# Kernel optimization log

Measured on AMD Instinct MI355X. Metric: run time of the kernel, lower is better.

Reference implementation:

```python
import jax, jax.numpy as jnp
import numpy as np
from jax import lax
from jax.scipy.linalg import cho_solve, solve_triangular

T_LEN, D, K = 8192, 32, 16
LOG2PI = float(np.log(2.0 * np.pi))


def setup_inputs():
    ks = jax.random.split(jax.random.key(0), 14)
    R = 0.1 * jax.random.normal(ks[0], (T_LEN, D, D))
    recog_J = jnp.einsum('tij,tkj->tik', R, R) + 0.5 * jnp.eye(D)  # SPD recognition precisions
    recog_h = 0.1 * jax.random.normal(ks[1], (T_LEN, D, 1))
    loc = 0.1 * jax.random.normal(ks[2], (D, 1))
    Tau_p = jnp.eye(D) + 0.05 * jax.random.normal(ks[3], (D, D))
    Lambda_p = jnp.eye(D) + 0.05 * jax.random.normal(ks[4], (D, D))
    X = 0.9 * jnp.eye(D, D + 1) + 0.05 * jax.random.normal(ks[5], (D, D + 1))
    init_lps = jax.nn.log_softmax(jax.random.normal(ks[6], (K,)))[:, None]
    trans_lps = jax.nn.log_softmax(jax.random.normal(ks[7], (K, K)), axis=1)
    Rp = 0.1 * jax.random.normal(ks[8], (K, D, D))
    prior_lam = jnp.einsum('kij,klj->kil', Rp, Rp) + jnp.eye(D)
    prior_X = 0.9 * jnp.eye(D, D + 1) + 0.05 * jax.random.normal(ks[9], (K, D, D + 1))
    Rt = 0.1 * jax.random.normal(ks[10], (D, D))
    prior_tau = Rt @ Rt.T + jnp.eye(D)
    prior_mu = 0.1 * jax.random.normal(ks[11], (D, 1))
    init_lps_prior = jax.nn.log_softmax(jax.random.normal(ks[12], (K,)))[:, None]
    trans_lps_prior = jax.nn.log_softmax(jax.random.normal(ks[13], (K, K)), axis=1)
    return dict(recog_J=recog_J, recog_h=recog_h, loc=loc, Tau_p=Tau_p, Lambda_p=Lambda_p, X=X,
                init_lps=init_lps, trans_lps=trans_lps, prior_lam=prior_lam, prior_X=prior_X,
                prior_tau=prior_tau, prior_mu=prior_mu, init_lps_prior=init_lps_prior,
                trans_lps_prior=trans_lps_prior, seed=42)


def _slds(recog_J, recog_h, loc, Tau_p, Lambda_p, X, init_lps, trans_lps,
          prior_lam, prior_X, prior_tau, prior_mu, init_lps_prior, trans_lps_prior, seed):
    Dd = loc.shape[0]
    Kk = init_lps.shape[0]
    Tt = recog_J.shape[0]
    Nn = Tt - 1
    eye = jnp.eye(Dd, dtype=recog_J.dtype)
    jitter = 1e-6 * eye

    # expected_params: inference LDS natural params
    tau = Tau_p @ Tau_p.T + 1e-8 * eye
    tau_mu = tau @ loc
    lam = Lambda_p @ Lambda_p.T + 1e-8 * eye
    A = X[:, :Dd]
    b = X[:, Dd:]
    ATlam = A.T @ lam
    ATlamA = ATlam @ A
    lamA = lam @ A
    lamb = lam @ b
    ATlamb = A.T @ lamb
    bTlamb = (b.T @ lamb)[0, 0]
    logdet_lam = jnp.linalg.slogdet(lam)[1]

    # ---- HMM forward-backward over z_{1:N} (emissions are zeros, kept general) ----
    emit = jnp.zeros((Nn, Kk), dtype=recog_J.dtype)

    def fstep(a, e):
        a2 = jax.nn.logsumexp(a[:, None] + trans_lps, axis=0) + e
        return a2, a2
    a0 = init_lps[:, 0] + emit[0]
    _, alphas_rest = lax.scan(fstep, a0, emit[1:])
    alphas = jnp.concatenate([a0[None], alphas_rest], 0)  # (N,K)
    hmm_logZ = jax.nn.logsumexp(alphas[-1])

    def bstep(beta_next, e_next):
        beta = jax.nn.logsumexp(trans_lps + (e_next + beta_next)[None, :], axis=1)
        return beta, beta
    _, betas_head = lax.scan(bstep, jnp.zeros(Kk, dtype=recog_J.dtype), emit[1:], reverse=True)
    betas = jnp.concatenate([betas_head, jnp.zeros((1, Kk), dtype=recog_J.dtype)], 0)
    cat_es = jnp.exp(alphas + betas - hmm_logZ)  # (N,K) marginals q(z_t)
    pair = jnp.exp(alphas[:-1, :, None] + trans_lps[None] + (emit[1:] + betas[1:])[:, None, :] - hmm_logZ)
    EZZNT = jnp.sum(pair, 0)  # (K,K) expected transition counts

    hmm_kl = (jnp.sum(cat_es[0] * (init_lps[:, 0] - init_lps_prior[:, 0]))
              + jnp.sum(EZZNT * (trans_lps - trans_lps_prior))
              + jnp.sum(cat_es * emit) - hmm_logZ)

    # ---- LDS information-form Kalman filter (computes logZ of q) ----
    J0 = tau + recog_J[0]
    h0 = tau_mu + recog_h[0]
    logc0 = -0.5 * (loc.T @ tau_mu)[0, 0] + 0.5 * jnp.linalg.slogdet(tau)[1] - 0.5 * Dd * LOG2PI

    def filt(carry, xs):
        J, h, lc = carry
        Jr, hr = xs
        M = J + ATlamA + jitter
        C = jnp.linalg.cholesky(M)
        u = h - ATlamb
        Minv_u = cho_solve((C, True), u)
        logdetM = 2.0 * jnp.sum(jnp.log(jnp.diagonal(C)))
        Jn = lam + Jr - lamA @ cho_solve((C, True), ATlam)
        hn = lamb + hr + lamA @ Minv_u
        lc = lc - 0.5 * bTlamb + 0.5 * logdet_lam + 0.5 * (u.T @ Minv_u)[0, 0] - 0.5 * logdetM
        return (Jn, hn, lc), (Jn, hn)

    (Jlast, hlast, logc), (Jf_rest, hf_rest) = lax.scan(filt, (J0, h0, logc0), (recog_J[1:], recog_h[1:]))
    Jf = jnp.concatenate([J0[None], Jf_rest], 0)  # (T,D,D) filtered precisions
    hf = jnp.concatenate([h0[None], hf_rest], 0)  # (T,D,1)
    Cl = jnp.linalg.cholesky(Jlast + jitter)
    mlast = cho_solve((Cl, True), hlast)
    logZq = logc + 0.5 * (hlast.T @ mlast)[0, 0] + 0.5 * Dd * LOG2PI - jnp.sum(jnp.log(jnp.diagonal(Cl)))

    # ---- RTS smoother -> gaussian expected stats ----
    CovT = cho_solve((Cl, True), eye)

    def smooth(carry, xs):
        m_n, Cov_n = carry
        Jt, ht = xs
        P = Jt + ATlamA + jitter
        C = jnp.linalg.cholesky(P)
        G = cho_solve((C, True), ATlam)
        g = cho_solve((C, True), ht - ATlamb)
        m = G @ m_n + g
        Pinv = cho_solve((C, True), eye)
        Cov = Pinv + G @ Cov_n @ G.T
        cross = G @ (Cov_n + m_n @ m_n.T) + g @ m_n.T  # E[x_t x_{t+1}^T]
        return (m, Cov), (m, Cov, cross)

    _, (m_head, Cov_head, cross) = lax.scan(smooth, (mlast, CovT), (Jf[:-1], hf[:-1]), reverse=True)
    Ex = jnp.concatenate([m_head, mlast[None]], 0)  # (T,D,1)
    Cov = jnp.concatenate([Cov_head, CovT[None]], 0)
    ExxT = Cov + jnp.einsum('tiz,tjz->tij', Ex, Ex)  # (T,D,D)
    Cross = jnp.swapaxes(cross, 1, 2)  # E[x_{t+1} x_t^T], (N,D,D)
    Ex2 = Ex[..., 0]

    # ---- E_q[log p_inf(x)] ----
    init_term = (-0.5 * jnp.einsum('ij,ij->', tau, ExxT[0]) + jnp.dot(Ex2[0], tau_mu[:, 0])
                 - 0.5 * (loc.T @ tau_mu)[0, 0] + 0.5 * jnp.linalg.slogdet(tau)[1] - 0.5 * Dd * LOG2PI)
    trans_term = (-0.5 * jnp.einsum('ij,nij->', lam, ExxT[1:])
                  + jnp.einsum('ij,nij->', lamA, Cross)
                  - 0.5 * jnp.einsum('ij,nij->', ATlamA, ExxT[:-1])
                  + jnp.einsum('i,ni->', lamb[:, 0], Ex2[1:])
                  - jnp.einsum('i,ni->', ATlamb[:, 0], Ex2[:-1])
                  + Nn * (-0.5 * bTlamb + 0.5 * logdet_lam - 0.5 * Dd * LOG2PI))
    E_log_p_inf = init_term + trans_term

    # ---- hmm_to_lds_mf: mixture (mean-field) prior expected log-density ----
    Ak = prior_X[:, :, :Dd]
    bk = prior_X[:, :, Dd:]
    lamAk = jnp.einsum('kij,kjl->kil', prior_lam, Ak)
    ATlamAk = jnp.einsum('kji,kjl->kil', Ak, lamAk)
    lambk = jnp.einsum('kij,kjz->kiz', prior_lam, bk)
    ATlambk = jnp.einsum('kji,kjz->kiz', Ak, lambk)
    bTlambk = jnp.einsum('kjz,kjz->k', bk, lambk)
    logdetk = jnp.linalg.slogdet(prior_lam)[1]
    w = cat_es  # (N,K)
    mix_trans = (-0.5 * jnp.einsum('nk,kij,nij->', w, prior_lam, ExxT[1:])
                 + jnp.einsum('nk,kij,nij->', w, lamAk, Cross)
                 - 0.5 * jnp.einsum('nk,kij,nij->', w, ATlamAk, ExxT[:-1])
                 + jnp.einsum('nk,ki,ni->', w, lambk[:, :, 0], Ex2[1:])
                 - jnp.einsum('nk,ki,ni->', w, ATlambk[:, :, 0], Ex2[:-1])
                 + jnp.einsum('nk,k->', w, -0.5 * bTlambk + 0.5 * logdetk)
                 - 0.5 * Nn * Dd * LOG2PI)
    tpm = prior_tau @ prior_mu
    mix_init = (-0.5 * jnp.einsum('ij,ij->', prior_tau, ExxT[0]) + jnp.dot(Ex2[0], tpm[:, 0])
                - 0.5 * (prior_mu.T @ tpm)[0, 0] + 0.5 * jnp.linalg.slogdet(prior_tau)[1] - 0.5 * Dd * LOG2PI)
    E_log_p_mix = mix_init + mix_trans

    recog_term = (-0.5 * jnp.einsum('tij,tij->', recog_J, ExxT)
                  + jnp.einsum('tiz,tiz->', recog_h, Ex))
    lds_kl = E_log_p_inf + recog_term - logZq - E_log_p_mix

    # ---- joint backward sampling of x_{1:T} ~ q ----
    eps = jax.random.normal(jax.random.fold_in(jax.random.key(seed), 1), (Tt, Dd, 1), dtype=recog_J.dtype)
    xT = mlast + solve_triangular(Cl.T, eps[-1], lower=False)

    def samp(x_next, xs):
        Jt, ht, e = xs
        P = Jt + ATlamA + jitter
        C = jnp.linalg.cholesky(P)
        mean = cho_solve((C, True), ht - ATlamb + ATlam @ x_next)
        x = mean + solve_triangular(C.T, e, lower=False)
        return x, x

    _, xs_head = lax.scan(samp, xT, (Jf[:-1], hf[:-1], eps[:-1]), reverse=True)
    z = jnp.concatenate([xs_head, xT[None]], 0)[..., 0]  # (T,D)

    return z, Ex, ExxT, Cross, cat_es, lds_kl + hmm_kl


def reference(recog_J, recog_h, loc, Tau_p, Lambda_p, X, init_lps, trans_lps,
              prior_lam, prior_X, prior_tau, prior_mu, init_lps_prior, trans_lps_prior, seed):
    return _slds(recog_J, recog_h, loc, Tau_p, Lambda_p, X, init_lps, trans_lps,
                 prior_lam, prior_X, prior_tau, prior_mu, init_lps_prior, trans_lps_prior, seed)
```

## Files before the change

### kernel.cpp

```cpp
#include <hip/hip_runtime.h>
#include <math.h>
#include <stdint.h>

#define Dd 32
#define TT 8192
#define NN 8191
#define KK 16
#define LOG2PI_ 1.8378770664093453

#define WSD_LOGC0  0
#define WSD_LOGZQ  1
#define WSD_MIXC   3
#define WSD_LDLAM  4
#define WSD_BTLAMB 5
#define WSD_PR     8
#define WSD_PT     1032
#define WSD_PM     2056
#define F_TAU      0
#define F_TAUMU    1024
#define F_LAM      1056
#define F_A        2080
#define F_B        3104
#define F_ATLAM    3136
#define F_ATLAMA   4160
#define F_LAMA     5184
#define F_LAMB     6208
#define F_ATLAMB   6240
#define F_SC       6272
#define F_LAMAK    6304
#define F_ATLAMAK  22688
#define F_LAMBK    39072
#define F_ATLAMBK  39584
#define F_BTLAMBK  40096
#define F_LOGDETK  40112
#define F_TPM      40128
#define F_J0       40160
#define F_H0       41184
#define F_MLAST    41216
#define F_COVT     41248
#define F_XT       42272
#define F_TPOW     42304
#define F_ALPHA    45632
#define F_BETA     176704
#define F_EZ       307776
#define F_SCAN     340544

#define SSTR   2148
#define POFF   0
#define QOFF   528
#define ROFF   1056
#define PPOFF  2080
#define QQOFF  2112
#define GAMOFF 2144
#define FLGOFF 2146
#define BG     0
#define BCZ    1024
#define BCM    1056
#define BP     1088

#define O_Z     ((size_t)0)
#define O_EX    ((size_t)262144)
#define O_EXXT  ((size_t)524288)
#define O_CROSS ((size_t)8912896)
#define O_CAT   ((size_t)17300480)
#define O_KL    ((size_t)17431536)

__device__ __forceinline__ uint32_t rotl32(uint32_t v, int d){ return (v<<d)|(v>>(32-d)); }
__device__ __forceinline__ void threefry2x32(uint32_t k0, uint32_t k1, uint32_t x0, uint32_t x1,
                                             uint32_t& o0, uint32_t& o1){
  uint32_t ks2 = k0 ^ k1 ^ 0x1BD11BDAu;
  x0 += k0; x1 += k1;
  x0+=x1; x1=rotl32(x1,13); x1^=x0;  x0+=x1; x1=rotl32(x1,15); x1^=x0;
  x0+=x1; x1=rotl32(x1,26); x1^=x0;  x0+=x1; x1=rotl32(x1, 6); x1^=x0;
  x0+=k1; x1+=ks2+1u;
  x0+=x1; x1=rotl32(x1,17); x1^=x0;  x0+=x1; x1=rotl32(x1,29); x1^=x0;
  x0+=x1; x1=rotl32(x1,16); x1^=x0;  x0+=x1; x1=rotl32(x1,24); x1^=x0;
  x0+=ks2; x1+=k0+2u;
  x0+=x1; x1=rotl32(x1,13); x1^=x0;  x0+=x1; x1=rotl32(x1,15); x1^=x0;
  x0+=x1; x1=rotl32(x1,26); x1^=x0;  x0+=x1; x1=rotl32(x1, 6); x1^=x0;
  x0+=k0; x1+=k1+3u;
  x0+=x1; x1=rotl32(x1,17); x1^=x0;  x0+=x1; x1=rotl32(x1,29); x1^=x0;
  x0+=x1; x1=rotl32(x1,16); x1^=x0;  x0+=x1; x1=rotl32(x1,24); x1^=x0;
  x0+=k1; x1+=ks2+4u;
  x0+=x1; x1=rotl32(x1,13); x1^=x0;  x0+=x1; x1=rotl32(x1,15); x1^=x0;
  x0+=x1; x1=rotl32(x1,26); x1^=x0;  x0+=x1; x1=rotl32(x1, 6); x1^=x0;
  x0+=ks2; x1+=k0+5u;
  o0=x0; o1=x1;
}
__device__ __forceinline__ float tf_normal(uint32_t bits){
  float fl = __uint_as_float((bits>>9) | 0x3F800000u) - 1.0f;
  const float lo = -0.99999994f;
  float u = fmaxf(lo, fl*2.0f + lo);
  float w = -log1pf(-u*u);
  float p;
  if (w < 5.0f){
    w -= 2.5f;
    p = 2.81022636e-08f;
    p = fmaf(p,w,3.43273939e-07f); p = fmaf(p,w,-3.5233877e-06f);
    p = fmaf(p,w,-4.39150654e-06f); p = fmaf(p,w,0.00021858087f);
    p = fmaf(p,w,-0.00125372503f); p = fmaf(p,w,-0.00417768164f);
    p = fmaf(p,w,0.246640727f); p = fmaf(p,w,1.50140941f);
  } else {
    w = sqrtf(w) - 3.0f;
    p = -0.000200214257f;
    p = fmaf(p,w,0.000100950558f); p = fmaf(p,w,0.00134934322f);
    p = fmaf(p,w,-0.00367342844f); p = fmaf(p,w,0.00573950773f);
    p = fmaf(p,w,-0.0076224613f); p = fmaf(p,w,0.00943887047f);
    p = fmaf(p,w,1.00167406f); p = fmaf(p,w,2.83297682f);
  }
  return 1.4142135381698608f * (p*u);
}

__device__ __forceinline__ void tri_rc(int i, int& r, int& c){
  int rr = (int)((sqrtf(8.f*(float)i+1.f)-1.f)*0.5f);
  while((rr+1)*(rr+2)/2 <= i) ++rr;
  while(rr*(rr+1)/2 > i) --rr;
  r = rr; c = i - rr*(rr+1)/2;
}

__device__ __forceinline__ float dot36(const float* A, int r, const float* B, int c){
  const float4* a4 = (const float4*)(A + r*36);
  const float4* b4 = (const float4*)(B + c*36);
  float sx=0.f, sy=0.f, sz=0.f, sw=0.f;
  #pragma unroll
  for(int m=0;m<8;++m){
    float4 a=a4[m], b=b4[m];
    sx=fmaf(a.x,b.x,sx); sy=fmaf(a.y,b.y,sy);
    sz=fmaf(a.z,b.z,sz); sw=fmaf(a.w,b.w,sw);
  }
  return (sx+sy)+(sz+sw);
}
__device__ __forceinline__ void t36_rows(float* dst, const float* src, int tid){
  int r=tid>>3, c0=(tid&7)<<2;
  *(float4*)(dst + r*36 + c0) = *(const float4*)(src + r*32 + c0);
}
__device__ __forceinline__ void t36_tr(float* dst, const float* src, int tid){
  int m=tid>>3, j0=(tid&7)<<2;
  float4 v = *(const float4*)(src + m*32 + j0);
  dst[(j0+0)*36+m]=v.x; dst[(j0+1)*36+m]=v.y;
  dst[(j0+2)*36+m]=v.z; dst[(j0+3)*36+m]=v.w;
}
__device__ __forceinline__ void t36_tr36(float* dst, const float* src, int tid){
  int m=tid>>3, j0=(tid&7)<<2;
  float4 v = *(const float4*)(src + m*36 + j0);
  dst[(j0+0)*36+m]=v.x; dst[(j0+1)*36+m]=v.y;
  dst[(j0+2)*36+m]=v.z; dst[(j0+3)*36+m]=v.w;
}
__device__ __forceinline__ void t36_sym(float* dst, const float* packed, int tid){
  for(int q=tid;q<528;q+=256){
    int r,c; tri_rc(q,r,c);
    float v=packed[q];
    dst[r*36+c]=v; dst[c*36+r]=v;
  }
}

__device__ double chol_linv36(float* W, float* Li, float* rdg, int tid){
  int r = tid>>3, c0 = (tid&7)<<2;
  {
    float4 z = make_float4(0.f,0.f,0.f,0.f);
    if(r>=c0 && r<c0+4) ((float*)&z)[r-c0]=1.f;
    *(float4*)(Li + r*36 + c0) = z;
  }
  double slog=0.0;
  for(int j=0;j<33;++j){
    if(j<32){
      float dd = W[j*36+j];
      float rd = 1.0f/sqrtf(dd);
      float invd = rd*rd;
      if(tid==0){ rdg[j]=rd; slog += (double)(0.5f*__logf(dd)); }
      if(r>j && c0+3>=j){
        float t0 = W[j*36+r]*invd;
        float4 wj  = *(const float4*)(W+j*36+c0);
        float4 cur = *(float4*)(W+r*36+c0);
        float rdl = rd;
        int c;
        c=c0;   cur.x = (c>j)? fmaf(-t0, wj.x, cur.x) : ((c==j)? cur.x*rdl : cur.x);
        c=c0+1; cur.y = (c>j)? fmaf(-t0, wj.y, cur.y) : ((c==j)? cur.y*rdl : cur.y);
        c=c0+2; cur.z = (c>j)? fmaf(-t0, wj.z, cur.z) : ((c==j)? cur.z*rdl : cur.z);
        c=c0+3; cur.w = (c>j)? fmaf(-t0, wj.w, cur.w) : ((c==j)? cur.w*rdl : cur.w);
        *(float4*)(W+r*36+c0) = cur;
      }
    }
    if(j>0){
      int ii=j-1;
      if(r>ii && c0<=ii){
        float wri = W[r*36+ii]*rdg[ii];
        float4 lrow = *(const float4*)(Li+ii*36+c0);
        float4 cur  = *(float4*)(Li+r*36+c0);
        if(c0+0<=ii) cur.x = fmaf(-wri, lrow.x, cur.x);
        if(c0+1<=ii) cur.y = fmaf(-wri, lrow.y, cur.y);
        if(c0+2<=ii) cur.z = fmaf(-wri, lrow.z, cur.z);
        if(c0+3<=ii) cur.w = fmaf(-wri, lrow.w, cur.w);
        *(float4*)(Li+r*36+c0) = cur;
      }
    }
    __syncthreads();
  }
  {
    float rr = rdg[r];
    float4 cur = *(float4*)(Li+r*36+c0);
    cur.x*=rr; cur.y*=rr; cur.z*=rr; cur.w*=rr;
    *(float4*)(Li+r*36+c0) = cur;
  }
  __syncthreads();
  return slog;
}

__device__ __forceinline__ double blk_red(double v, double* sd, int tid){
  sd[tid]=v; __syncthreads();
  for(int s=128;s>0;s>>=1){ if(tid<s) sd[tid]+=sd[tid+s]; __syncthreads(); }
  double r=sd[0]; __syncthreads(); return r;
}
__device__ double blk_logdet(float* Ms, int tid){
  double sl = 0.0;
  for (int j=0;j<Dd;++j){
    float dd = Ms[j*33+j];
    sl += log((double)dd);
    float invd = 1.0f/dd;
    #pragma unroll
    for(int p=0;p<4;p++){
      int cell = tid + (p<<8); int r=cell>>5, c=cell&31;
      if(r>j && c>j && c<=r) Ms[r*33+c] -= Ms[r*33+j]*(Ms[c*33+j]*invd);
    }
    __syncthreads();
  }
  return sl;
}

__device__ void gen_leaf(float* S, int s, const float* rJ, const float* rh,
                         const float* wsf, const double* wsd, int tid){
  if(s==0){
    #pragma unroll 3
    for(int q=tid;q<528;q+=256){
      int r,c; tri_rc(q,r,c);
      S[POFF+q]=0.f;
      S[QOFF+q]=wsf[F_J0 + r*32+c];
    }
    #pragma unroll 4
    for(int q=tid;q<1024;q+=256) S[ROFF+q]=0.f;
    if(tid<32){ S[PPOFF+tid]=0.f; S[QQOFF+tid]=wsf[F_H0+tid]; }
    if(tid==0){ *(double*)(S+GAMOFF)=wsd[WSD_LOGC0]; S[FLGOFF]=1.f; }
  } else {
    #pragma unroll 3
    for(int q=tid;q<528;q+=256){
      int r,c; tri_rc(q,r,c);
      S[POFF+q] = wsf[F_ATLAMA + r*32+c] + ((r==c)?1e-6f:0.f);
      S[QOFF+q] = wsf[F_LAM + r*32+c] + rJ[(size_t)s*1024 + r*32+c];
    }
    #pragma unroll 4
    for(int q=tid;q<1024;q+=256) S[ROFF+q] = -wsf[F_ATLAM+q];
    if(tid<32){
      S[PPOFF+tid] = -wsf[F_ATLAMB+tid];
      S[QQOFF+tid] = wsf[F_LAMB+tid] + rh[(size_t)s*32+tid];
    }
    if(tid==0){
      *(double*)(S+GAMOFF) = -0.5*wsd[WSD_BTLAMB] + 0.5*wsd[WSD_LDLAM];
      S[FLGOFF]=1.f;
    }
  }
}

__global__ __launch_bounds__(256) void k_setup(const float* rJ, const float* rh, const float* loc,
    const float* Tp, const float* Lp, const float* X, const float* plam, const float* pX,
    const float* ptau, const float* pmu, float* wsf, double* wsd){
  __shared__ float s1[1056], s2[1056], s3[1056];
  __shared__ float sv[32], sv2[32];
  int tid=threadIdx.x; int b=blockIdx.x;
  if(b==0){
    for(int p=0;p<4;p++){int cell=tid+(p<<8);int r=cell>>5,c=cell&31; s1[r*33+c]=Tp[cell];}
    if(tid<32) sv[tid]=loc[tid];
    __syncthreads();
    for(int p=0;p<4;p++){int cell=tid+(p<<8);int r=cell>>5,c=cell&31;
      float a=0.f;
      #pragma unroll
      for(int m=0;m<Dd;++m) a=fmaf(s1[r*33+m], s1[c*33+m], a);
      if(r==c) a+=1e-8f;
      s2[r*33+c]=a; wsf[F_TAU+cell]=a; wsf[F_J0+cell]=a+rJ[cell];
    }
    __syncthreads();
    if(tid<32){ float tm=0.f;
      #pragma unroll
      for(int m=0;m<Dd;++m) tm=fmaf(s2[tid*33+m], sv[m], tm);
      sv2[tid]=tm; wsf[F_TAUMU+tid]=tm; wsf[F_H0+tid]=tm+rh[tid];
    }
    __syncthreads();
    double ldt = blk_logdet(s2, tid);
    if(tid==0){ double dd=0; for(int m=0;m<Dd;++m) dd += (double)sv[m]*(double)sv2[m];
      wsd[WSD_LOGC0] = -0.5*dd + 0.5*ldt - 0.5*Dd*LOG2PI_; }
  } else if(b==1){
    for(int p=0;p<4;p++){int cell=tid+(p<<8);int r=cell>>5,c=cell&31; s1[r*33+c]=Lp[cell];}
    __syncthreads();
    for(int p=0;p<4;p++){int cell=tid+(p<<8);int r=cell>>5,c=cell&31;
      float a=0.f;
      #pragma unroll
      for(int m=0;m<Dd;++m) a=fmaf(s1[r*33+m], s1[c*33+m], a);
      if(r==c) a+=1e-8f;
      s2[r*33+c]=a; wsf[F_LAM+cell]=a;
    }
    __syncthreads();
    for(int p=0;p<4;p++){int cell=tid+(p<<8);int r=cell>>5,c=cell&31;
      float a=X[r*33+c]; s3[r*33+c]=a; wsf[F_A+cell]=a; }
    if(tid<32){ sv[tid]=X[tid*33+32]; wsf[F_B+tid]=sv[tid]; }
    __syncthreads();
    for(int p=0;p<4;p++){int cell=tid+(p<<8);int r=cell>>5,c=cell&31;
      float a=0.f,b2=0.f;
      #pragma unroll
      for(int m=0;m<Dd;++m){ a=fmaf(s2[r*33+m], s3[m*33+c], a); b2=fmaf(s3[m*33+r], s2[m*33+c], b2); }
      s1[r*33+c]=a; wsf[F_LAMA+cell]=a; wsf[F_ATLAM+cell]=b2;
    }
    if(tid<32){ float lb=0.f;
      #pragma unroll
      for(int m=0;m<Dd;++m) lb=fmaf(s2[tid*33+m], sv[m], lb);
      sv2[tid]=lb; wsf[F_LAMB+tid]=lb;
    }
    __syncthreads();
    for(int p=0;p<4;p++){int cell=tid+(p<<8);int r=cell>>5,c=cell&31;
      float a=0.f;
      #pragma unroll
      for(int m=0;m<Dd;++m) a=fmaf(s3[m*33+r], s1[m*33+c], a);
      wsf[F_ATLAMA+cell]=a;
    }
    if(tid<32){ float ab=0.f;
      #pragma unroll
      for(int m=0;m<Dd;++m) ab=fmaf(s3[m*33+tid], sv2[m], ab);
      wsf[F_ATLAMB+tid]=ab;
    }
    if(tid==0){ double bb=0; for(int m=0;m<Dd;++m) bb += (double)sv[m]*(double)sv2[m];
      wsd[WSD_BTLAMB]=bb; }
    __syncthreads();
    double ldl = blk_logdet(s2, tid);
    if(tid==0) wsd[WSD_LDLAM]=ldl;
  } else if(b==2){
    for(int p=0;p<4;p++){int cell=tid+(p<<8);int r=cell>>5,c=cell&31; s1[r*33+c]=ptau[cell];}
    if(tid<32) sv[tid]=pmu[tid];
    __syncthreads();
    if(tid<32){ float tm=0.f;
      #pragma unroll
      for(int m=0;m<Dd;++m) tm=fmaf(s1[tid*33+m], sv[m], tm);
      sv2[tid]=tm; wsf[F_TPM+tid]=tm;
    }
    __syncthreads();
    double ldp = blk_logdet(s1, tid);
    if(tid==0){ double dd=0; for(int m=0;m<Dd;++m) dd += (double)sv[m]*(double)sv2[m];
      wsd[WSD_MIXC] = -0.5*dd + 0.5*ldp - 0.5*Dd*LOG2PI_; }
  } else {
    int k2 = b-3;
    for(int p=0;p<4;p++){int cell=tid+(p<<8);int r=cell>>5,c=cell&31;
      s2[r*33+c]=plam[k2*1024+cell]; s3[r*33+c]=pX[k2*1056 + r*33 + c];}
    if(tid<32) sv[tid]=pX[k2*1056 + tid*33 + 32];
    __syncthreads();
    for(int p=0;p<4;p++){int cell=tid+(p<<8);int r=cell>>5,c=cell&31;
      float a=0.f;
      #pragma unroll
      for(int m=0;m<Dd;++m) a=fmaf(s2[r*33+m], s3[m*33+c], a);
      s1[r*33+c]=a; wsf[F_LAMAK + (size_t)k2*1024 + cell]=a;
    }
    if(tid<32){ float lb=0.f;
      #pragma unroll
      for(int m=0;m<Dd;++m) lb=fmaf(s2[tid*33+m], sv[m], lb);
      sv2[tid]=lb; wsf[F_LAMBK + k2*32 + tid]=lb;
    }
    __syncthreads();
    for(int p=0;p<4;p++){int cell=tid+(p<<8);int r=cell>>5,c=cell&31;
      float a=0.f;
      #pragma unroll
      for(int m=0;m<Dd;++m) a=fmaf(s3[m*33+r], s1[m*33+c], a);
      wsf[F_ATLAMAK + (size_t)k2*1024 + cell]=a;
    }
    if(tid<32){ float ab=0.f;
      #pragma unroll
      for(int m=0;m<Dd;++m) ab=fmaf(s3[m*33+tid], sv2[m], ab);
      wsf[F_ATLAMBK + k2*32 + tid]=ab;
    }
    if(tid==0){ float bb=0.f; for(int m=0;m<Dd;++m) bb=fmaf(sv[m],sv2[m],bb);
      wsf[F_BTLAMBK + k2]=bb; }
    __syncthreads();
    double dk = blk_logdet(s2, tid);
    if(tid==0) wsf[F_LOGDETK + k2]=(float)dk;
  }
}

__global__ __launch_bounds__(256) void k_eps(const int* seedp, float* outz){
  uint32_t seed = (uint32_t)seedp[0];
  uint32_t K0,K1;
  threefry2x32(0u, seed, 0u, 1u, K0, K1);
  uint32_t i = blockIdx.x*256u + threadIdx.x;
  uint32_t o0,o1;
  threefry2x32(K0, K1, 0u, i, o0, o1);
  outz[i] = tf_normal(o0 ^ o1);
}

__global__ __launch_bounds__(256) void k_hmmpow(const float* tl, float* wsf){
  __shared__ float A0[256], A1[256];
  int tid=threadIdx.x;
  A0[tid]=tl[tid];
  wsf[F_TPOW+tid]=A0[tid];
  __syncthreads();
  float* cur=A0; float* nxt=A1;
  for(int k=1;k<13;++k){
    int i=tid>>4, j=tid&15;
    float mx=-3.0e38f;
    #pragma unroll
    for(int m=0;m<16;++m) mx=fmaxf(mx, cur[i*16+m]+cur[m*16+j]);
    float s=0.f;
    #pragma unroll
    for(int m=0;m<16;++m) s+=__expf(cur[i*16+m]+cur[m*16+j]-mx);
    float v=mx+__logf(s);
    nxt[tid]=v; wsf[F_TPOW+k*256+tid]=v;
    __syncthreads();
    float* t2=cur; cur=nxt; nxt=t2;
  }
}

__global__ __launch_bounds__(256) void k_hmmab(const float* il, float* wsf){
  __shared__ float S[3328];
  int tid=threadIdx.x;
  for(int p=0;p<13;++p) S[p*256+tid]=wsf[F_TPOW+p*256+tid];
  __syncthreads();
  int n = blockIdx.x*256 + tid;
  if(n>NN-1) return;
  float v[16], w[16];
  #pragma unroll
  for(int j=0;j<16;++j) v[j]=il[j];
  for(int k=0;k<13;++k){
    if((n>>k)&1){
      #pragma unroll
      for(int j=0;j<16;++j){
        float mx=-3.0e38f;
        #pragma unroll
        for(int i2=0;i2<16;++i2) mx=fmaxf(mx, v[i2]+S[k*256+i2*16+j]);
        float s=0.f;
        #pragma unroll
        for(int i2=0;i2<16;++i2) s+=__expf(v[i2]+S[k*256+i2*16+j]-mx);
        w[j]=mx+__logf(s);
      }
      #pragma unroll
      for(int j=0;j<16;++j) v[j]=w[j];
    }
  }
  #pragma unroll
  for(int j=0;j<16;++j) wsf[F_ALPHA+(size_t)n*16+j]=v[j];
  if(n==NN-1){
    float mx=-3.0e38f;
    #pragma unroll
    for(int j=0;j<16;++j) mx=fmaxf(mx,v[j]);
    float s=0.f;
    #pragma unroll
    for(int j=0;j<16;++j) s+=__expf(v[j]-mx);
    wsf[F_SC+0]=mx+__logf(s);
  }
  int m = NN-1-n;
  float b[16];
  #pragma unroll
  for(int i2=0;i2<16;++i2) b[i2]=0.f;
  for(int k=0;k<13;++k){
    if((m>>k)&1){
      #pragma unroll
      for(int i2=0;i2<16;++i2){
        float mx=-3.0e38f;
        #pragma unroll
        for(int j=0;j<16;++j) mx=fmaxf(mx, S[k*256+i2*16+j]+b[j]);
        float s=0.f;
        #pragma unroll
        for(int j=0;j<16;++j) s+=__expf(S[k*256+i2*16+j]+b[j]-mx);
        w[i2]=mx+__logf(s);
      }
      #pragma unroll
      for(int i2=0;i2<16;++i2) b[i2]=w[i2];
    }
  }
  #pragma unroll
  for(int i2=0;i2<16;++i2) wsf[F_BETA+(size_t)n*16+i2]=b[i2];
}

__global__ __launch_bounds__(256) void k_cat(const float* tl, float* wsf, float* out){
  __shared__ float Ts[256]; __shared__ float al[1024]; __shared__ float be[1040];
  int tid=threadIdx.x;
  Ts[tid]=tl[tid];
  float logZ = wsf[F_SC+0];
  int n0=blockIdx.x*64;
  for(int q=tid;q<1024;q+=256){ int n=n0+(q>>4); al[q] = (n<NN)? wsf[F_ALPHA+(size_t)n*16+(q&15)] : 0.f; }
  for(int q=tid;q<1040;q+=256){ int n=n0+(q>>4); be[q] = (n<NN)? wsf[F_BETA +(size_t)n*16+(q&15)] : 0.f; }
  __syncthreads();
  for(int q=tid;q<1024;q+=256){ int n=n0+(q>>4);
    if(n<NN) out[O_CAT+(size_t)n*16+(q&15)] = __expf(al[q]+be[q]-logZ); }
  int i=tid>>4, j=tid&15;
  float acc=0.f;
  #pragma unroll 4
  for(int nn=0;nn<64;++nn){
    int n=n0+nn;
    if(n<NN-1) acc += __expf(al[nn*16+i]+Ts[i*16+j]+be[(nn+1)*16+j]-logZ);
  }
  wsf[F_EZ + blockIdx.x*256 + tid]=acc;
}

__global__ __launch_bounds__(256,4) void k_cf(const float* rJ, const float* rh,
    float* wsf, double* wsd, float* out, int d, int mode){
  __shared__ __align__(16) float SA[2148], SB[2148];
  __shared__ __align__(16) float W[1152], Li[1152], BA[1152], BB[1152];
  __shared__ float rdg[32], Ls[32];
  int tid = threadIdx.x;
  int i = blockIdx.x;
  int iA = (i<<(d+1)) + (1<<d) - 1;
  int iB = iA + (1<<d);
  float* base = wsf + F_SCAN;
  float* pa = base + (size_t)iA*SSTR;
  float* pb = base + (size_t)iB*SSTR;
  if(d==0){
    gen_leaf(SA, iA, rJ, rh, wsf, wsd, tid);
    if(mode==0) gen_leaf(SB, iB, rJ, rh, wsf, wsd, tid);
    else { 
      #pragma unroll 3
      for(int q=tid;q<537;q+=256) ((float4*)SB)[q]=((const float4*)pb)[q];
    }
  } else {
    #pragma unroll 3
    for(int q=tid;q<537;q+=256){ ((float4*)SA)[q]=((const float4*)pa)[q]; ((float4*)SB)[q]=((const float4*)pb)[q]; }
  }
  __syncthreads();
  int fa=(SA[FLGOFF]!=0.f), fb=(SB[FLGOFF]!=0.f);
  if(mode==1){
    float* st = out + O_EXXT;
    #pragma unroll 3
    for(int q=tid;q<537;q+=256){ ((float4*)st)[q]=((float4*)SB)[q]; ((float4*)pb)[q]=((float4*)SA)[q]; }
    if(tid==0) pa[FLGOFF]=0.f;
    return;
  }
  if(mode==2){
    #pragma unroll 3
    for(int q=tid;q<537;q+=256) ((float4*)pa)[q]=((float4*)SB)[q];
  }
  float* X = (mode==2)? SB : SA;  int fx=(mode==2)?fb:fa;
  float* Y = (mode==2)? SA : SB;  int fy=(mode==2)?fa:fb;
  if(!fx && !fy){ if(tid==0) pb[FLGOFF]=0.f; return; }
  if(!fx){ 
    #pragma unroll 3
    for(int q=tid;q<537;q+=256) ((float4*)pb)[q]=((float4*)Y)[q]; return; }
  if(!fy){ 
    #pragma unroll 3
    for(int q=tid;q<537;q+=256) ((float4*)pb)[q]=((float4*)X)[q]; return; }
  #pragma unroll 3
  for(int q=tid;q<528;q+=256){
    int r,c; tri_rc(q,r,c);
    float w = X[QOFF+q] + Y[POFF+q];
    W[r*36+c]=w; W[c*36+r]=w;
  }
  t36_rows(BA, X+ROFF, tid);
  t36_tr  (BB, Y+ROFF, tid);
  __syncthreads();
  double slog = chol_linv36(W, Li, rdg, tid);
  if(tid<32){
    float acc=0.f;
    for(int m=0;m<=tid;++m) acc = fmaf(Li[tid*36+m], X[QQOFF+m]+Y[PPOFF+m], acc);
    Ls[tid]=acc;
  }
  #pragma unroll 4
  for(int q=tid;q<1024;q+=256){
    int i2=q>>5, j=q&31;
    W[j*36+i2] = dot36(Li, i2, BA, j);
  }
  __syncthreads();
  #pragma unroll 4
  for(int q=tid;q<1024;q+=256){
    int i2=q>>5, j=q&31;
    BA[j*36+i2] = dot36(Li, i2, BB, j);
  }
  __syncthreads();
  #pragma unroll 3
  for(int q=tid;q<528;q+=256){
    int r,c; tri_rc(q,r,c);
    pb[POFF+q] = X[POFF+q] - dot36(W, r, W, c);
    pb[QOFF+q] = Y[QOFF+q] - dot36(BA, r, BA, c);
  }
  #pragma unroll 4
  for(int q=tid;q<1024;q+=256){
    int r=q>>5, c=q&31;
    pb[ROFF+q] = -dot36(W, r, BA, c);
  }
  if(tid<32){
    float ap=0.f,aq=0.f;
    #pragma unroll
    for(int m=0;m<32;++m){ ap=fmaf(W[tid*36+m],Ls[m],ap); aq=fmaf(BA[tid*36+m],Ls[m],aq); }
    pb[PPOFF+tid] = X[PPOFF+tid] - ap;
    pb[QQOFF+tid] = Y[QQOFF+tid] - aq;
  }
  if(tid==0){
    double g = *(double*)(X+GAMOFF) + *(double*)(Y+GAMOFF);
    double dot=0.0;
    for(int m=0;m<32;++m) dot += (double)Ls[m]*(double)Ls[m];
    *(double*)(pb+GAMOFF) = g + 0.5*dot - slog;
    pb[FLGOFF]=1.f;
  }
}

__global__ __launch_bounds__(256,6) void k_point(float* wsf, double* wsd, float* out){
  __shared__ __align__(16) float SE[2148];
  __shared__ __align__(16) float W[1152], Li[1152], AUX[1152];
  __shared__ float rdg[32], uv[32], Lu[32], ev[32], gv[32], yv[32];
  int tid=threadIdx.x; int b=blockIdx.x;
  float* base = wsf + F_SCAN;
  float* outz = out + O_Z;
  if(b>0){
    int t = b-1;
    float* pe = base + (size_t)b*SSTR;
    #pragma unroll 3
    for(int q=tid;q<537;q+=256) ((float4*)SE)[q]=((const float4*)pe)[q];
    if(tid<32) ev[tid]=outz[(size_t)t*32+tid];
    t36_rows(AUX, wsf+F_LAMA, tid);
    __syncthreads();
    #pragma unroll 3
    for(int q=tid;q<528;q+=256){
      int r,c; tri_rc(q,r,c);
      float w = SE[QOFF+q] + wsf[F_ATLAMA + r*32+c] + ((r==c)?1e-6f:0.f);
      W[r*36+c]=w; W[c*36+r]=w;
    }
    if(tid<32) uv[tid]=SE[QQOFF+tid]-wsf[F_ATLAMB+tid];
    __syncthreads();
    chol_linv36(W, Li, rdg, tid);
    if(tid<32){
      float acc=0.f;
      for(int m=0;m<=tid;++m) acc=fmaf(Li[tid*36+m],uv[m],acc);
      Lu[tid]=acc;
    }
    #pragma unroll 4
    for(int q=tid;q<1024;q+=256){
      int i2=q>>5, j=q&31;
      W[j*36+i2] = dot36(Li, i2, AUX, j);
    }
    __syncthreads();
    t36_tr36(AUX, Li, tid);
    if(tid<32){
      float ag=0.f, ay=0.f;
      for(int m2=tid;m2<32;++m2){ float lv=Li[m2*36+tid]; ag=fmaf(lv,Lu[m2],ag); ay=fmaf(lv,ev[m2],ay); }
      gv[tid]=ag; yv[tid]=ay;
    }
    __syncthreads();
    #pragma unroll 4
    for(int q=tid;q<1024;q+=256){
      int r=q>>5,c=q&31;
      pe[BG+q] = dot36(AUX, r, W, c);
    }
    float* outc = out + O_CROSS + (size_t)t*1024;
    #pragma unroll 3
    for(int q=tid;q<528;q+=256){
      int r,c; tri_rc(q,r,c);
      float a = dot36(AUX, r, AUX, c);
      pe[BP+q]=a; outc[q]=a;
    }
    if(tid<32){
      pe[BCM+tid]=gv[tid]; pe[BCZ+tid]=gv[tid]+yv[tid]; outc[528+tid]=gv[tid];
    }
    if(tid==0) pe[FLGOFF]=1.f;
  } else {
    const float* st = out + O_EXXT;
    #pragma unroll 3
    for(int q=tid;q<537;q+=256) ((float4*)SE)[q]=((const float4*)st)[q];
    if(tid<32) ev[tid]=outz[(size_t)NN*32+tid];
    __syncthreads();
    for(int q=tid;q<528;q+=256){
      int r,c; tri_rc(q,r,c);
      float w = SE[QOFF+q] + ((r==c)?1e-6f:0.f);
      W[r*36+c]=w; W[c*36+r]=w;
    }
    if(tid<32) uv[tid]=SE[QQOFF+tid];
    __syncthreads();
    double slog2 = chol_linv36(W, Li, rdg, tid);
    if(tid<32){
      float acc=0.f;
      for(int m=0;m<=tid;++m) acc=fmaf(Li[tid*36+m],uv[m],acc);
      Lu[tid]=acc;
    }
    t36_tr36(AUX, Li, tid);
    __syncthreads();
    if(tid<32){
      float am=0.f, ay=0.f;
      for(int m2=tid;m2<32;++m2){ float lv=Li[m2*36+tid]; am=fmaf(lv,Lu[m2],am); ay=fmaf(lv,ev[m2],ay); }
      gv[tid]=am; yv[tid]=ay;
      wsf[F_MLAST+tid]=am; out[O_EX+(size_t)NN*32+tid]=am;
      float xt=am+ay;
      wsf[F_XT+tid]=xt; out[O_Z+(size_t)NN*32+tid]=xt;
    }
    __syncthreads();
    for(int q=tid;q<1024;q+=256){
      int r=q>>5,c=q&31;
      float a = dot36(AUX, r, AUX, c);
      wsf[F_COVT+q]=a;
      out[O_EXXT+(size_t)NN*1024+q]=a+gv[r]*gv[c];
    }
    if(tid==0){
      double gam=*(const double*)(SE+GAMOFF);
      double hm=0.0;
      for(int m=0;m<32;++m) hm += (double)uv[m]*(double)gv[m];
      wsd[WSD_LOGZQ] = gam + 0.5*hm + 0.5*Dd*LOG2PI_ - slog2;
    }
  }
}

__device__ __forceinline__ int amap(int j){ return (j<NN)? (NN-j) : 0; }

__global__ __launch_bounds__(256,4) void k_ca(float* wsf, int d, int mode){
  __shared__ __align__(16) float SA[2148], SB[2148];
  __shared__ __align__(16) float GY36[1152], GB[1152], PX36[1152];
  int tid = threadIdx.x;
  int i = blockIdx.x;
  int iA = (i<<(d+1)) + (1<<d) - 1;
  int iB = iA + (1<<d);
  float* base = wsf + F_SCAN;
  float* pa = base + (size_t)amap(iA)*SSTR;
  float* pb = base + (size_t)amap(iB)*SSTR;
  #pragma unroll 3
  for(int q=tid;q<537;q+=256){ ((float4*)SA)[q]=((const float4*)pa)[q]; ((float4*)SB)[q]=((const float4*)pb)[q]; }
  __syncthreads();
  int fa=(SA[FLGOFF]!=0.f), fb=(SB[FLGOFF]!=0.f);
  if(mode==1){
    #pragma unroll 3
    for(int q=tid;q<537;q+=256) ((float4*)pb)[q]=((float4*)SA)[q];
    if(tid==0) pa[FLGOFF]=0.f;
    return;
  }
  if(mode==2){
    #pragma unroll 3
    for(int q=tid;q<537;q+=256) ((float4*)pa)[q]=((float4*)SB)[q];
  }
  float* X = (mode==2)? SB : SA;  int fx=(mode==2)?fb:fa;
  float* Y = (mode==2)? SA : SB;  int fy=(mode==2)?fa:fb;
  if(!fx && !fy){ if(tid==0) pb[FLGOFF]=0.f; return; }
  if(!fx){ 
    #pragma unroll 3
    for(int q=tid;q<537;q+=256) ((float4*)pb)[q]=((float4*)Y)[q]; return; }
  if(!fy){ 
    #pragma unroll 3
    for(int q=tid;q<537;q+=256) ((float4*)pb)[q]=((float4*)X)[q]; return; }
  t36_rows(GY36, Y+BG, tid);
  t36_tr  (GB,   X+BG, tid);
  t36_sym (PX36, X+BP, tid);
  __syncthreads();
  #pragma unroll 4
  for(int q=tid;q<1024;q+=256){
    int r=q>>5,c=q&31;
    pb[BG+q] = dot36(GY36, r, GB, c);
  }
  __syncthreads();
  #pragma unroll 4
  for(int q=tid;q<1024;q+=256){
    int r=q>>5,c=q&31;
    GB[r*36+c] = dot36(GY36, r, PX36, c);
  }
  __syncthreads();
  #pragma unroll 3
  for(int q=tid;q<528;q+=256){
    int r,c; tri_rc(q,r,c);
    pb[BP+q] = dot36(GB, r, GY36, c) + Y[BP+q];
  }
  if(tid<32){
    float az=0.f,am=0.f;
    #pragma unroll
    for(int m=0;m<32;++m){ float g=GY36[tid*36+m]; az=fmaf(g,X[BCZ+m],az); am=fmaf(g,X[BCM+m],am); }
    pb[BCZ+tid]=az+Y[BCZ+tid];
    pb[BCM+tid]=am+Y[BCM+tid];
  }
  if(tid==0) pb[FLGOFF]=1.f;
}

__global__ __launch_bounds__(256,6) void k_smz(float* wsf, float* out){
  __shared__ __align__(16) float G36[1152], CV36[1152], Tm36[1152];
  __shared__ float mlv[32], xtv[32], mv[32], zv[32];
  int tid=threadIdx.x;
  int t = blockIdx.x;
  const float* pe = wsf + F_SCAN + (size_t)t*SSTR;
  t36_rows(G36,  pe+BG,       tid);
  t36_rows(CV36, wsf+F_COVT,  tid);
  if(tid<32){ mlv[tid]=wsf[F_MLAST+tid]; xtv[tid]=wsf[F_XT+tid]; }
  __syncthreads();
  if(tid<32){
    float am=0.f, az=0.f;
    #pragma unroll
    for(int m=0;m<32;++m){
      float g=G36[tid*36+m];
      am=fmaf(g, mlv[m], am);
      az=fmaf(g, xtv[m], az);
    }
    mv[tid]=am+pe[BCM+tid];
    zv[tid]=az+pe[BCZ+tid];
    out[O_EX+(size_t)t*32+tid]=mv[tid];
    out[O_Z +(size_t)t*32+tid]=zv[tid];
  }
  #pragma unroll 4
  for(int q=tid;q<1024;q+=256){
    int r=q>>5,c=q&31;
    Tm36[r*36+c] = dot36(G36, r, CV36, c);
  }
  __syncthreads();
  #pragma unroll 3
  for(int q=tid;q<528;q+=256){
    int r,c; tri_rc(q,r,c);
    float cov = dot36(Tm36, r, G36, c) + pe[BP+q];
    float e = cov + mv[r]*mv[c];
    out[O_EXXT+(size_t)t*1024 + r*32+c]=e;
    if(r!=c) out[O_EXXT+(size_t)t*1024 + c*32+r]=e;
  }
}

__global__ __launch_bounds__(256,6) void k_cross(float* wsf, float* out){
  __shared__ __align__(16) float PV36[1152], LA36[1152], E136[1152], GF36[1152];
  __shared__ float gv[32], m1[32];
  int tid=threadIdx.x;
  int t = blockIdx.x;
  float* outc = out + O_CROSS + (size_t)t*1024;
  t36_sym (PV36, outc, tid);
  t36_rows(LA36, wsf+F_LAMA, tid);
  t36_rows(E136, out+O_EXXT+(size_t)(t+1)*1024, tid);
  if(tid<32){ gv[tid]=outc[528+tid]; m1[tid]=out[O_EX+(size_t)(t+1)*32+tid]; }
  __syncthreads();
  #pragma unroll 4
  for(int q=tid;q<1024;q+=256){
    int r=q>>5,c=q&31;
    GF36[r*36+c] = dot36(PV36, r, LA36, c);
  }
  __syncthreads();
  #pragma unroll 4
  for(int q=tid;q<1024;q+=256){
    int i2=q>>5, j=q&31;
    float acc = dot36(GF36, j, E136, i2);
    outc[q] = acc + gv[j]*m1[i2];
  }
}

__global__ __launch_bounds__(256) void k_terms(const float* rJ, const float* rh,
    const float* plam, float* wsf, double* wsd, float* out){
  __shared__ float slam[1056], slamA[1056], sata[1056];
  __shared__ float slamb[32], satlb[32], cst[16], sw[16];
  __shared__ double sd[256];
  int tid=threadIdx.x; int i8=tid>>3, c4=(tid&7)*4;
  for(int p=0;p<4;p++){int cell=tid+(p<<8);int r=cell>>5,c=cell&31;
    slam[r*33+c]=wsf[F_LAM+cell]; slamA[r*33+c]=wsf[F_LAMA+cell]; sata[r*33+c]=wsf[F_ATLAMA+cell];}
  if(tid<32){slamb[tid]=wsf[F_LAMB+tid]; satlb[tid]=wsf[F_ATLAMB+tid];}
  if(tid<16) cst[tid] = -0.5f*wsf[F_BTLAMBK+tid] + 0.5f*wsf[F_LOGDETK+tid];
  __syncthreads();
  double dr=0.0, dt=0.0, dm=0.0;
  int t0=blockIdx.x*8;
  for(int tt=0;tt<8;++tt){
    int t=t0+tt;
    if(t<NN){ if(tid<16) sw[tid]=out[O_CAT+(size_t)t*16+tid]; }
    __syncthreads();
    size_t cb=(size_t)t*1024+((size_t)i8<<5)+c4;
    float4 exT=*(const float4*)(out+O_EXXT+cb);
    float4 rj =*(const float4*)(rJ+cb);
    dr += -0.5*(double)(rj.x*exT.x+rj.y*exT.y+rj.z*exT.z+rj.w*exT.w);
    if(tid<32) dr += (double)(rh[(size_t)t*32+tid]*out[O_EX+(size_t)t*32+tid]);
    if(t>=1){
      dt += -0.5*(double)(slam[i8*33+c4]*exT.x + slam[i8*33+c4+1]*exT.y
                        + slam[i8*33+c4+2]*exT.z + slam[i8*33+c4+3]*exT.w);
      if(tid<32) dt += (double)(slamb[tid]*out[O_EX+(size_t)t*32+tid]);
    }
    if(t<NN){
      float4 crT =*(const float4*)(out+O_CROSS+cb);
      float4 exT1=*(const float4*)(out+O_EXXT+cb+1024);
      dt += (double)(slamA[i8*33+c4]*crT.x + slamA[i8*33+c4+1]*crT.y
                   + slamA[i8*33+c4+2]*crT.z + slamA[i8*33+c4+3]*crT.w)
          -0.5*(double)(sata[i8*33+c4]*exT.x + sata[i8*33+c4+1]*exT.y
                      + sata[i8*33+c4+2]*exT.z + sata[i8*33+c4+3]*exT.w);
      if(tid<32) dt -= (double)(satlb[tid]*out[O_EX+(size_t)t*32+tid]);
      const float* pe1=(const float*)&exT1; const float* pcr=(const float*)&crT; const float* pe0=(const float*)&exT;
      #pragma unroll
      for(int q=0;q<4;q++){
        int cc=(i8<<5)+c4+q;
        float wl=0.f, wa=0.f, wt2=0.f;
        #pragma unroll
        for(int k2=0;k2<KK;k2++){ float wv=sw[k2];
          wl =fmaf(wv, plam[(size_t)k2*1024+cc], wl);
          wa =fmaf(wv, wsf[F_LAMAK+(size_t)k2*1024+cc], wa);
          wt2=fmaf(wv, wsf[F_ATLAMAK+(size_t)k2*1024+cc], wt2);}
        dm += (double)(-0.5f*wl*pe1[q] + wa*pcr[q] - 0.5f*wt2*pe0[q]);
      }
      if(tid<32){
        float wlb=0.f, wtb=0.f;
        #pragma unroll
        for(int k2=0;k2<KK;k2++){ wlb=fmaf(sw[k2], wsf[F_LAMBK+k2*32+tid], wlb);
                                  wtb=fmaf(sw[k2], wsf[F_ATLAMBK+k2*32+tid], wtb);}
        dm += (double)(wlb*out[O_EX+(size_t)(t+1)*32+tid] - wtb*out[O_EX+(size_t)t*32+tid]);
      }
      if(tid<16) dm += (double)(sw[tid]*cst[tid]);
    }
    __syncthreads();
  }
  double r1=blk_red(dr,sd,tid);
  double r2=blk_red(dt,sd,tid);
  double r3=blk_red(dm,sd,tid);
  if(tid==0){ wsd[WSD_PR+blockIdx.x]=r1; wsd[WSD_PT+blockIdx.x]=r2; wsd[WSD_PM+blockIdx.x]=r3; }
}

__global__ __launch_bounds__(256) void k_final(const float* il, const float* tl,
    const float* ilp, const float* tlp, const float* ptau, float* wsf, double* wsd, float* out){
  __shared__ double sd[256];
  int tid=threadIdx.x;
  double ez=0.0;
  for(int b=0;b<128;++b) ez += (double)wsf[F_EZ + b*256 + tid];
  double v = ez * (double)(tl[tid]-tlp[tid]);
  if(tid<16) v += (double)out[O_CAT+tid] * (double)(il[tid]-ilp[tid]);
  double hmmkl = blk_red(v, sd, tid) - (double)wsf[F_SC+0];
  double a=0,b2=0,c=0;
  for(int q=0;q<4;q++){int b3=tid+q*256; a+=wsd[WSD_PR+b3]; b2+=wsd[WSD_PT+b3]; c+=wsd[WSD_PM+b3];}
  double recog=blk_red(a,sd,tid), trns=blk_red(b2,sd,tid), mixt=blk_red(c,sd,tid);
  double ia=0, ib=0, va=0, vb=0;
  for(int p=0;p<4;p++){int cell=tid+(p<<8);
    float e0=out[O_EXXT+cell];
    ia += (double)(wsf[F_TAU+cell]*e0);
    ib += (double)(ptau[cell]*e0);
  }
  if(tid<32){ float ex0=out[O_EX+tid];
    va=(double)(ex0*wsf[F_TAUMU+tid]); vb=(double)(ex0*wsf[F_TPM+tid]); }
  double s_ia=blk_red(ia,sd,tid), s_ib=blk_red(ib,sd,tid);
  double s_va=blk_red(va,sd,tid), s_vb=blk_red(vb,sd,tid);
  if(tid==0){
    double init_term = -0.5*s_ia + s_va + wsd[WSD_LOGC0];
    double mix_init  = -0.5*s_ib + s_vb + wsd[WSD_MIXC];
    double trans_term = trns + (double)NN*(-0.5*wsd[WSD_BTLAMB] + 0.5*wsd[WSD_LDLAM] - 0.5*Dd*LOG2PI_);
    double mix_trans  = mixt - 0.5*(double)NN*(double)Dd*LOG2PI_;
    double lds_kl = (init_term+trans_term) + recog - wsd[WSD_LOGZQ] - (mix_init+mix_trans);
    out[O_KL] = (float)(lds_kl + hmmkl);
  }
}

extern "C" void kernel_launch(void* const* d_in, const int* in_sizes, int n_in,
                              void* d_out, int out_size, void* d_ws, size_t ws_size,
                              hipStream_t stream){
  const float* rJ  =(const float*)d_in[0];
  const float* rh  =(const float*)d_in[1];
  const float* loc =(const float*)d_in[2];
  const float* Tp  =(const float*)d_in[3];
  const float* Lp  =(const float*)d_in[4];
  const float* X   =(const float*)d_in[5];
  const float* il  =(const float*)d_in[6];
  const float* tl  =(const float*)d_in[7];
  const float* plam=(const float*)d_in[8];
  const float* pX  =(const float*)d_in[9];
  const float* ptau=(const float*)d_in[10];
  const float* pmu =(const float*)d_in[11];
  const float* ilp =(const float*)d_in[12];
  const float* tlp =(const float*)d_in[13];
  const int*   seed=(const int*)d_in[14];
  float* out=(float*)d_out;
  double* wsd=(double*)d_ws;
  float* wsf=(float*)((char*)d_ws + 32768);

  k_setup<<<19,256,0,stream>>>(rJ,rh,loc,Tp,Lp,X,plam,pX,ptau,pmu,wsf,wsd);
  k_eps<<<1024,256,0,stream>>>(seed, out + O_Z);
  k_hmmpow<<<1,256,0,stream>>>(tl, wsf);
  k_hmmab<<<32,256,0,stream>>>(il, wsf);
  k_cat<<<128,256,0,stream>>>(tl, wsf, out);
  for(int d=0; d<13; ++d) k_cf<<<(8192>>(d+1)),256,0,stream>>>(rJ, rh, wsf, wsd, out, d, 0);
  k_cf<<<1,256,0,stream>>>(rJ, rh, wsf, wsd, out, 12, 1);
  for(int d=11; d>=0; --d) k_cf<<<(8192>>(d+1)),256,0,stream>>>(rJ, rh, wsf, wsd, out, d, 2);
  k_point<<<8192,256,0,stream>>>(wsf, wsd, out);
  for(int d=0; d<13; ++d) k_ca<<<(8192>>(d+1)),256,0,stream>>>(wsf, d, 0);
  k_ca<<<1,256,0,stream>>>(wsf, 12, 1);
  for(int d=11; d>=0; --d) k_ca<<<(8192>>(d+1)),256,0,stream>>>(wsf, d, 2);
  k_smz<<<NN,256,0,stream>>>(wsf, out);
  k_cross<<<NN,256,0,stream>>>(wsf, out);
  k_terms<<<1024,256,0,stream>>>(rJ, rh, plam, wsf, wsd, out);
  k_final<<<1,256,0,stream>>>(il, tl, ilp, tlp, ptau, wsf, wsd, out);
}
```

Before: 2.077 ms.

## Replace tree scans with chunked three-level blocked scans for filter and smoother

Replaces the up-sweep/down-sweep tree parallel scans (about 25 launches each) for the forward filter and the backward smoother with a blocked scan. Each block first sequentially combines a chunk of 8 elements, then two reduction levels and a single-block exclusive scan of 16 hyper-aggregates run, and finally the prefixes propagate back down. The point-wise k_point and k_smz kernels are fused into the propagation kernels, and scratch prefixes are staged in the O_CROSS output region. This cuts launch count and global traffic but serialises more work per block, with fewer blocks at the middle levels.

```diff
diff --git a/kernel.cpp b/kernel.cpp
--- a/kernel.cpp
+++ b/kernel.cpp
@@ -65,6 +65,10 @@
 #define O_CAT   ((size_t)17300480)
 #define O_KL    ((size_t)17431536)
 
+#define SAGG0  0
+#define SSUP0  1024
+#define SHYP0  1152
+
 __device__ __forceinline__ uint32_t rotl32(uint32_t v, int d){ return (v<<d)|(v>>(32-d)); }
 __device__ __forceinline__ void threefry2x32(uint32_t k0, uint32_t k1, uint32_t x0, uint32_t x1,
                                              uint32_t& o0, uint32_t& o1){
@@ -154,6 +158,29 @@
   }
 }
 
+__device__ __forceinline__ void ld_slot(float* dst, const float* src, int tid){
+  #pragma unroll 3
+  for(int q=tid;q<537;q+=256) ((float4*)dst)[q] = ((const float4*)src)[q];
+}
+__device__ __forceinline__ void st_slot(float* dst, const float* src, int tid){
+  #pragma unroll 3
+  for(int q=tid;q<537;q+=256) ((float4*)dst)[q] = ((const float4*)src)[q];
+}
+__device__ __forceinline__ void st_pref(float* cb, int p, const float* C, int tid){
+  #pragma unroll 3
+  for(int q=tid;q<537;q+=256){
+    int w=q/116, o=(q-116*w)<<2;
+    *(float4*)(cb + (((size_t)(5*p+w))<<10) + 560 + o) = ((const float4*)C)[q];
+  }
+}
+__device__ __forceinline__ void ld_pref(float* C, const float* cb, int p, int tid){
+  #pragma unroll 3
+  for(int q=tid;q<537;q+=256){
+    int w=q/116, o=(q-116*w)<<2;
+    ((float4*)C)[q] = *(const float4*)(cb + (((size_t)(5*p+w))<<10) + 560 + o);
+  }
+}
+
 __device__ double chol_linv36(float* W, float* Li, float* rdg, int tid){
   int r = tid>>3, c0 = (tid&7)<<2;
   {
@@ -227,37 +254,235 @@
   return sl;
 }
 
-__device__ void gen_leaf(float* S, int s, const float* rJ, const float* rh,
-                         const float* wsf, const double* wsd, int tid){
-  if(s==0){
+__device__ void unary_f(float* C, const float* wsf, const double* wsd, int tid){
+  __syncthreads();
+  #pragma unroll 3
+  for(int q=tid;q<528;q+=256){
+    int r,c; tri_rc(q,r,c);
+    C[POFF+q]=0.f;
+    C[QOFF+q]=wsf[F_J0 + r*32+c];
+  }
+  #pragma unroll 4
+  for(int q=tid;q<1024;q+=256) C[ROFF+q]=0.f;
+  if(tid<32){ C[PPOFF+tid]=0.f; C[QQOFF+tid]=wsf[F_H0+tid]; }
+  if(tid==0){ *(double*)(C+GAMOFF)=wsd[WSD_LOGC0]; C[FLGOFF]=1.f; }
+}
+__device__ void leaf_f(float* C, int t, const float* rJ, const float* rh,
+                       const float* wsf, const double* wsd, int tid){
+  __syncthreads();
+  #pragma unroll 3
+  for(int q=tid;q<528;q+=256){
+    int r,c; tri_rc(q,r,c);
+    C[POFF+q] = wsf[F_ATLAMA + r*32+c] + ((r==c)?1e-6f:0.f);
+    C[QOFF+q] = wsf[F_LAM + r*32+c] + rJ[(size_t)t*1024 + r*32+c];
+  }
+  #pragma unroll 4
+  for(int q=tid;q<1024;q+=256) C[ROFF+q] = -wsf[F_ATLAM+q];
+  if(tid<32){
+    C[PPOFF+tid] = -wsf[F_ATLAMB+tid];
+    C[QQOFF+tid] = wsf[F_LAMB+tid] + rh[(size_t)t*32+tid];
+  }
+  if(tid==0){
+    *(double*)(C+GAMOFF) = -0.5*wsd[WSD_BTLAMB] + 0.5*wsd[WSD_LDLAM];
+    C[FLGOFF]=1.f;
+  }
+}
+
+__device__ void comb_f(float* C, const float* Y, float* W, float* Li, float* BA, float* BB,
+                       float* rdg, float* Ls, int tid){
+  __syncthreads();
+  int fc=(C[FLGOFF]!=0.f), fy=(Y[FLGOFF]!=0.f);
+  if(fy && !fc){
+    #pragma unroll 3
+    for(int q=tid;q<537;q+=256) ((float4*)C)[q]=((const float4*)Y)[q];
+  } else if(fy){
     #pragma unroll 3
     for(int q=tid;q<528;q+=256){
       int r,c; tri_rc(q,r,c);
-      S[POFF+q]=0.f;
-      S[QOFF+q]=wsf[F_J0 + r*32+c];
+      float w = C[QOFF+q] + Y[POFF+q];
+      W[r*36+c]=w; W[c*36+r]=w;
+    }
+    t36_rows(BA, C+ROFF, tid);
+    t36_tr  (BB, Y+ROFF, tid);
+    __syncthreads();
+    double slog = chol_linv36(W, Li, rdg, tid);
+    if(tid<32){
+      float acc=0.f;
+      for(int m=0;m<=tid;++m) acc=fmaf(Li[tid*36+m], C[QQOFF+m]+Y[PPOFF+m], acc);
+      Ls[tid]=acc;
     }
     #pragma unroll 4
-    for(int q=tid;q<1024;q+=256) S[ROFF+q]=0.f;
-    if(tid<32){ S[PPOFF+tid]=0.f; S[QQOFF+tid]=wsf[F_H0+tid]; }
-    if(tid==0){ *(double*)(S+GAMOFF)=wsd[WSD_LOGC0]; S[FLGOFF]=1.f; }
-  } else {
+    for(int q=tid;q<1024;q+=256){ int i2=q>>5, j=q&31; W[j*36+i2]=dot36(Li,i2,BA,j); }
+    __syncthreads();
+    #pragma unroll 4
+    for(int q=tid;q<1024;q+=256){ int i2=q>>5, j=q&31; BA[j*36+i2]=dot36(Li,i2,BB,j); }
+    __syncthreads();
     #pragma unroll 3
     for(int q=tid;q<528;q+=256){
       int r,c; tri_rc(q,r,c);
-      S[POFF+q] = wsf[F_ATLAMA + r*32+c] + ((r==c)?1e-6f:0.f);
-      S[QOFF+q] = wsf[F_LAM + r*32+c] + rJ[(size_t)s*1024 + r*32+c];
+      C[POFF+q] = C[POFF+q] - dot36(W,r,W,c);
+      C[QOFF+q] = Y[QOFF+q] - dot36(BA,r,BA,c);
     }
     #pragma unroll 4
-    for(int q=tid;q<1024;q+=256) S[ROFF+q] = -wsf[F_ATLAM+q];
+    for(int q=tid;q<1024;q+=256){ int r=q>>5,c=q&31; C[ROFF+q] = -dot36(W,r,BA,c); }
     if(tid<32){
-      S[PPOFF+tid] = -wsf[F_ATLAMB+tid];
-      S[QQOFF+tid] = wsf[F_LAMB+tid] + rh[(size_t)s*32+tid];
+      float ap=0.f,aq=0.f;
+      #pragma unroll
+      for(int m=0;m<32;++m){ ap=fmaf(W[tid*36+m],Ls[m],ap); aq=fmaf(BA[tid*36+m],Ls[m],aq); }
+      C[PPOFF+tid] -= ap;
+      C[QQOFF+tid] = Y[QQOFF+tid] - aq;
     }
     if(tid==0){
-      *(double*)(S+GAMOFF) = -0.5*wsd[WSD_BTLAMB] + 0.5*wsd[WSD_LDLAM];
-      S[FLGOFF]=1.f;
-    }
-  }
+      double g = *(double*)(C+GAMOFF) + *(const double*)(Y+GAMOFF);
+      double dot=0.0;
+      for(int m=0;m<32;++m) dot += (double)Ls[m]*(double)Ls[m];
+      *(double*)(C+GAMOFF) = g + 0.5*dot - slog;
+    }
+  }
+  __syncthreads();
+}
+
+template<int POINT>
+__device__ void adv_leaf_f(float* C, int t, const float* rJ, const float* rh,
+                           const float* wsf, const double* wsd,
+                           const float* CLAMA, const float* CATA, const float* catb,
+                           float* W, float* Li, float* BA, float* BB,
+                           float* rdg, float* Lu, float* uv, float* ev,
+                           float* pe, float* outc, const float* outz, int tid){
+  __syncthreads();
+  #pragma unroll 3
+  for(int q=tid;q<528;q+=256){
+    int r,c; tri_rc(q,r,c);
+    float w = C[QOFF+q] + CATA[r*36+c];
+    W[r*36+c]=w; W[c*36+r]=w;
+  }
+  t36_rows(BB, C+ROFF, tid);
+  if(tid<32){
+    uv[tid] = C[QQOFF+tid] - catb[tid];
+    if(POINT) ev[tid] = outz[(size_t)(t-1)*32+tid];
+  }
+  __syncthreads();
+  double slog = chol_linv36(W, Li, rdg, tid);
+  if(tid<32){
+    float acc=0.f;
+    for(int m=0;m<=tid;++m) acc=fmaf(Li[tid*36+m], uv[m], acc);
+    Lu[tid]=acc;
+  }
+  #pragma unroll 4
+  for(int q=tid;q<1024;q+=256){ int i2=q>>5, j=q&31; W[j*36+i2]=dot36(Li,i2,BB,j); }
+  __syncthreads();
+  #pragma unroll 4
+  for(int q=tid;q<1024;q+=256){ int i2=q>>5, j=q&31; BA[j*36+i2]=dot36(Li,i2,CLAMA,j); }
+  __syncthreads();
+  if(POINT){
+    t36_tr36(BB, Li, tid);
+    __syncthreads();
+    #pragma unroll 4
+    for(int q=tid;q<1024;q+=256){ int r=q>>5,c=q&31; pe[BG+q]=dot36(BB,r,BA,c); }
+    #pragma unroll 3
+    for(int q=tid;q<528;q+=256){ int r,c; tri_rc(q,r,c); float a=dot36(BB,r,BB,c); pe[BP+q]=a; outc[q]=a; }
+    if(tid<32){
+      float ag=0.f, ay=0.f;
+      for(int m2=tid;m2<32;++m2){ float lv=Li[m2*36+tid]; ag=fmaf(lv,Lu[m2],ag); ay=fmaf(lv,ev[m2],ay); }
+      pe[BCM+tid]=ag; pe[BCZ+tid]=ag+ay; outc[528+tid]=ag;
+    }
+    if(tid==0) pe[FLGOFF]=1.f;
+  }
+  #pragma unroll 3
+  for(int q=tid;q<528;q+=256){
+    int r,c; tri_rc(q,r,c);
+    C[POFF+q] = C[POFF+q] - dot36(W,r,W,c);
+    C[QOFF+q] = (wsf[F_LAM + r*32+c] + rJ[(size_t)t*1024 + r*32+c]) - dot36(BA,r,BA,c);
+  }
+  #pragma unroll 4
+  for(int q=tid;q<1024;q+=256){ int r=q>>5,c=q&31; C[ROFF+q] = dot36(W,r,BA,c); }
+  if(tid<32){
+    float ap=0.f,aq=0.f;
+    #pragma unroll
+    for(int m=0;m<32;++m){ ap=fmaf(W[tid*36+m],Lu[m],ap); aq=fmaf(BA[tid*36+m],Lu[m],aq); }
+    C[PPOFF+tid] -= ap;
+    C[QQOFF+tid] = (wsf[F_LAMB+tid] + rh[(size_t)t*32+tid]) + aq;
+  }
+  if(tid==0){
+    double dot=0.0;
+    for(int m=0;m<32;++m) dot += (double)Lu[m]*(double)Lu[m];
+    *(double*)(C+GAMOFF) += (-0.5*wsd[WSD_BTLAMB] + 0.5*wsd[WSD_LDLAM]) + 0.5*dot - slog;
+  }
+}
+
+__device__ void final_f(float* C, float* W, float* Li, float* BB,
+                        float* rdg, float* Lu, float* uv, float* ev, float* gv,
+                        float* wsf, double* wsd, float* out, int tid){
+  __syncthreads();
+  #pragma unroll 3
+  for(int q=tid;q<528;q+=256){
+    int r,c; tri_rc(q,r,c);
+    float w = C[QOFF+q] + ((r==c)?1e-6f:0.f);
+    W[r*36+c]=w; W[c*36+r]=w;
+  }
+  if(tid<32){ uv[tid]=C[QQOFF+tid]; ev[tid]=out[O_Z+(size_t)NN*32+tid]; }
+  __syncthreads();
+  double slog2 = chol_linv36(W, Li, rdg, tid);
+  if(tid<32){
+    float acc=0.f;
+    for(int m=0;m<=tid;++m) acc=fmaf(Li[tid*36+m], uv[m], acc);
+    Lu[tid]=acc;
+  }
+  t36_tr36(BB, Li, tid);
+  __syncthreads();
+  if(tid<32){
+    float am=0.f, ay=0.f;
+    for(int m2=tid;m2<32;++m2){ float lv=Li[m2*36+tid]; am=fmaf(lv,Lu[m2],am); ay=fmaf(lv,ev[m2],ay); }
+    gv[tid]=am;
+    wsf[F_MLAST+tid]=am; out[O_EX+(size_t)NN*32+tid]=am;
+    float xt=am+ay;
+    wsf[F_XT+tid]=xt; out[O_Z+(size_t)NN*32+tid]=xt;
+  }
+  __syncthreads();
+  #pragma unroll 4
+  for(int q=tid;q<1024;q+=256){
+    int r=q>>5,c=q&31;
+    float a = dot36(BB,r,BB,c);
+    wsf[F_COVT+q]=a;
+    out[O_EXXT+(size_t)NN*1024+q]=a+gv[r]*gv[c];
+  }
+  if(tid==0){
+    double gam=*(double*)(C+GAMOFF);
+    double hm=0.0;
+    for(int m=0;m<32;++m) hm += (double)uv[m]*(double)gv[m];
+    wsd[WSD_LOGZQ] = gam + 0.5*hm + 0.5*Dd*LOG2PI_ - slog2;
+  }
+}
+
+__device__ void comb_a(float* C, const float* Y, float* B1, float* B2, float* B3, float* B4,
+                       float* vcz, float* vcm, int tid){
+  __syncthreads();
+  int fc=(C[FLGOFF]!=0.f), fy=(Y[FLGOFF]!=0.f);
+  if(fy && !fc){
+    #pragma unroll 3
+    for(int q=tid;q<537;q+=256) ((float4*)C)[q]=((const float4*)Y)[q];
+  } else if(fy){
+    t36_rows(B1, Y+BG, tid);
+    t36_tr  (B3, C+BG, tid);
+    t36_sym (B4, C+BP, tid);
+    if(tid<32){ vcz[tid]=C[BCZ+tid]; vcm[tid]=C[BCM+tid]; }
+    __syncthreads();
+    #pragma unroll 4
+    for(int q=tid;q<1024;q+=256){ int r=q>>5,c=q&31; C[BG+q]=dot36(B1,r,B3,c); }
+    #pragma unroll 4
+    for(int q=tid;q<1024;q+=256){ int r=q>>5,c=q&31; B2[r*36+c]=dot36(B1,r,B4,c); }
+    __syncthreads();
+    #pragma unroll 3
+    for(int q=tid;q<528;q+=256){ int r,c; tri_rc(q,r,c); C[BP+q]=dot36(B2,r,B1,c)+Y[BP+q]; }
+    if(tid<32){
+      float az=0.f,am=0.f;
+      #pragma unroll
+      for(int m=0;m<32;++m){ float g=B1[tid*36+m]; az=fmaf(g,vcz[m],az); am=fmaf(g,vcm[m],am); }
+      C[BCZ+tid]=az+Y[BCZ+tid];
+      C[BCM+tid]=am+Y[BCM+tid];
+    }
+  }
+  __syncthreads();
 }
 
 __global__ __launch_bounds__(256) void k_setup(const float* rJ, const float* rh, const float* loc,
@@ -494,310 +719,191 @@
   wsf[F_EZ + blockIdx.x*256 + tid]=acc;
 }
 
-__global__ __launch_bounds__(256,4) void k_cf(const float* rJ, const float* rh,
-    float* wsf, double* wsd, float* out, int d, int mode){
-  __shared__ __align__(16) float SA[2148], SB[2148];
+__global__ __launch_bounds__(256,4) void kf_agg(const float* rJ, const float* rh,
+                                                float* wsf, double* wsd, float* out){
+  __shared__ __align__(16) float C[2148];
+  __shared__ __align__(16) float W[1152], Li[1152], BA[1152], BB[1152], CLAMA[1152], CATA[1152];
+  __shared__ float rdg[32], Lu[32], uv[32], ev[32], catb[32];
+  int tid=threadIdx.x; int i=blockIdx.x;
+  if(i==0 && tid==0) wsf[F_SCAN+FLGOFF]=0.f;
+  t36_rows(CLAMA, wsf+F_LAMA, tid);
+  for(int q=tid;q<528;q+=256){ int r,c; tri_rc(q,r,c);
+    float v=wsf[F_ATLAMA+r*32+c]+((r==c)?1e-6f:0.f); CATA[r*36+c]=v; CATA[c*36+r]=v; }
+  if(tid<32) catb[tid]=wsf[F_ATLAMB+tid];
+  if(i==0) unary_f(C, wsf, wsd, tid);
+  else     leaf_f(C, 8*i, rJ, rh, wsf, wsd, tid);
+  for(int e=1;e<8;++e)
+    adv_leaf_f<0>(C, 8*i+e, rJ, rh, wsf, wsd, CLAMA, CATA, catb,
+                  W,Li,BA,BB, rdg,Lu,uv,ev, (float*)0, (float*)0, (const float*)0, tid);
+  __syncthreads();
+  st_pref(out + O_CROSS, SAGG0+i, C, tid);
+}
+
+__global__ __launch_bounds__(256,4) void kf_seq(float* out, int in0, int out0){
+  __shared__ __align__(16) float C[2148], Y[2148];
   __shared__ __align__(16) float W[1152], Li[1152], BA[1152], BB[1152];
   __shared__ float rdg[32], Ls[32];
-  int tid = threadIdx.x;
-  int i = blockIdx.x;
-  int iA = (i<<(d+1)) + (1<<d) - 1;
-  int iB = iA + (1<<d);
-  float* base = wsf + F_SCAN;
-  float* pa = base + (size_t)iA*SSTR;
-  float* pb = base + (size_t)iB*SSTR;
-  if(d==0){
-    gen_leaf(SA, iA, rJ, rh, wsf, wsd, tid);
-    if(mode==0) gen_leaf(SB, iB, rJ, rh, wsf, wsd, tid);
-    else { 
+  int tid=threadIdx.x; int i=blockIdx.x;
+  float* cb = out + O_CROSS;
+  ld_pref(C, cb, in0+8*i, tid);
+  for(int e=1;e<8;++e){
+    ld_pref(Y, cb, in0+8*i+e, tid);
+    comb_f(C, Y, W,Li,BA,BB, rdg,Ls, tid);
+  }
+  __syncthreads();
+  st_pref(cb, out0+i, C, tid);
+}
+__global__ __launch_bounds__(256,4) void kf_sqx(float* out, int base, int n){
+  __shared__ __align__(16) float C[2148], Y[2148];
+  __shared__ __align__(16) float W[1152], Li[1152], BA[1152], BB[1152];
+  __shared__ float rdg[32], Ls[32];
+  int tid=threadIdx.x;
+  float* cb = out + O_CROSS;
+  if(tid==0) C[FLGOFF]=0.f;
+  for(int e=0;e<n;++e){
+    ld_pref(Y, cb, base+e, tid);
+    __syncthreads();
+    st_pref(cb, base+e, C, tid);
+    comb_f(C, Y, W,Li,BA,BB, rdg,Ls, tid);
+  }
+}
+__global__ __launch_bounds__(256,4) void kf_sqp(float* out, int pre0, int el0){
+  __shared__ __align__(16) float C[2148], Y[2148];
+  __shared__ __align__(16) float W[1152], Li[1152], BA[1152], BB[1152];
+  __shared__ float rdg[32], Ls[32];
+  int tid=threadIdx.x; int i=blockIdx.x;
+  float* cb = out + O_CROSS;
+  ld_pref(C, cb, pre0+i, tid);
+  for(int e=0;e<8;++e){
+    ld_pref(Y, cb, el0+8*i+e, tid);
+    __syncthreads();
+    st_pref(cb, el0+8*i+e, C, tid);
+    comb_f(C, Y, W,Li,BA,BB, rdg,Ls, tid);
+  }
+}
+
+__global__ __launch_bounds__(256,4) void kf_prop(const float* rJ, const float* rh,
+                                                 float* wsf, double* wsd, float* out){
+  __shared__ __align__(16) float C[2148];
+  __shared__ __align__(16) float W[1152], Li[1152], BA[1152], BB[1152], CLAMA[1152], CATA[1152];
+  __shared__ float rdg[32], Lu[32], uv[32], ev[32], catb[32], gv[32];
+  int tid=threadIdx.x; int i=blockIdx.x;
+  float* cb = out + O_CROSS;
+  ld_pref(C, cb, SAGG0+i, tid);
+  t36_rows(CLAMA, wsf+F_LAMA, tid);
+  for(int q=tid;q<528;q+=256){ int r,c; tri_rc(q,r,c);
+    float v=wsf[F_ATLAMA+r*32+c]+((r==c)?1e-6f:0.f); CATA[r*36+c]=v; CATA[c*36+r]=v; }
+  if(tid<32) catb[tid]=wsf[F_ATLAMB+tid];
+  for(int e=0;e<8;++e){
+    int j=8*i+e;
+    if(j==0){
+      unary_f(C, wsf, wsd, tid);
+    } else {
+      adv_leaf_f<1>(C, j, rJ, rh, wsf, wsd, CLAMA, CATA, catb,
+                    W,Li,BA,BB, rdg,Lu,uv,ev,
+                    wsf + F_SCAN + (size_t)j*SSTR,
+                    out + O_CROSS + (size_t)(j-1)*1024,
+                    out + O_Z, tid);
+    }
+  }
+  if(i==1023) final_f(C, W,Li,BB, rdg,Lu,uv,ev,gv, wsf, wsd, out, tid);
+}
+
+__global__ __launch_bounds__(256,4) void ka_agg(float* wsf, float* out){
+  __shared__ __align__(16) float C[2148], Y[2148];
+  __shared__ __align__(16) float B1[1152], B2[1152], B3[1152], B4[1152];
+  __shared__ float vcz[32], vcm[32];
+  int tid=threadIdx.x; int i=blockIdx.x;
+  ld_slot(C, wsf + F_SCAN + (size_t)(NN-8*i)*SSTR, tid);
+  for(int e=1;e<8;++e){
+    int j=8*i+e; int s=(j<NN)? (NN-j) : 0;
+    ld_slot(Y, wsf + F_SCAN + (size_t)s*SSTR, tid);
+    comb_a(C, Y, B1,B2,B3,B4, vcz,vcm, tid);
+  }
+  __syncthreads();
+  st_pref(out + O_CROSS, SAGG0+i, C, tid);
+}
+
+__global__ __launch_bounds__(256,4) void ka_seq(float* out, int in0, int out0){
+  __shared__ __align__(16) float C[2148], Y[2148];
+  __shared__ __align__(16) float B1[1152], B2[1152], B3[1152], B4[1152];
+  __shared__ float vcz[32], vcm[32];
+  int tid=threadIdx.x; int i=blockIdx.x;
+  float* cb = out + O_CROSS;
+  ld_pref(C, cb, in0+8*i, tid);
+  for(int e=1;e<8;++e){
+    ld_pref(Y, cb, in0+8*i+e, tid);
+    comb_a(C, Y, B1,B2,B3,B4, vcz,vcm, tid);
+  }
+  __syncthreads();
+  st_pref(cb, out0+i, C, tid);
+}
+__global__ __launch_bounds__(256,4) void ka_sqx(float* out, int base, int n){
+  __shared__ __align__(16) float C[2148], Y[2148];
+  __shared__ __align__(16) float B1[1152], B2[1152], B3[1152], B4[1152];
+  __shared__ float vcz[32], vcm[32];
+  int tid=threadIdx.x;
+  float* cb = out + O_CROSS;
+  if(tid==0) C[FLGOFF]=0.f;
+  for(int e=0;e<n;++e){
+    ld_pref(Y, cb, base+e, tid);
+    __syncthreads();
+    st_pref(cb, base+e, C, tid);
+    comb_a(C, Y, B1,B2,B3,B4, vcz,vcm, tid);
+  }
+}
+__global__ __launch_bounds__(256,4) void ka_sqp(float* out, int pre0, int el0){
+  __shared__ __align__(16) float C[2148], Y[2148];
+  __shared__ __align__(16) float B1[1152], B2[1152], B3[1152], B4[1152];
+  __shared__ float vcz[32], vcm[32];
+  int tid=threadIdx.x; int i=blockIdx.x;
+  float* cb = out + O_CROSS;
+  ld_pref(C, cb, pre0+i, tid);
+  for(int e=0;e<8;++e){
+    ld_pref(Y, cb, el0+8*i+e, tid);
+    __syncthreads();
+    st_pref(cb, el0+8*i+e, C, tid);
+    comb_a(C, Y, B1,B2,B3,B4, vcz,vcm, tid);
+  }
+}
+
+__global__ __launch_bounds__(256,4) void ka_prop(float* wsf, float* out){
+  __shared__ __align__(16) float C[2148], Y[2148];
+  __shared__ __align__(16) float B1[1152], B2[1152], B3[1152], B4[1152];
+  __shared__ float vcz[32], vcm[32], mlv[32], xtv[32], mv[32];
+  int tid=threadIdx.x; int i=blockIdx.x;
+  ld_pref(C, out + O_CROSS, SAGG0+i, tid);
+  if(tid<32){ mlv[tid]=wsf[F_MLAST+tid]; xtv[tid]=wsf[F_XT+tid]; }
+  __syncthreads();
+  for(int e=0;e<8;++e){
+    int j=8*i+e;
+    if(j>0){
+      int t=NN-j;
+      t36_rows(B1, C+BG, tid);
+      t36_rows(B4, wsf+F_COVT, tid);
+      __syncthreads();
+      if(tid<32){
+        float am=0.f, az=0.f;
+        #pragma unroll
+        for(int m=0;m<32;++m){ float g=B1[tid*36+m]; am=fmaf(g,mlv[m],am); az=fmaf(g,xtv[m],az); }
+        mv[tid]=am+C[BCM+tid];
+        out[O_EX+(size_t)t*32+tid]=mv[tid];
+        out[O_Z +(size_t)t*32+tid]=az+C[BCZ+tid];
+      }
+      #pragma unroll 4
+      for(int q=tid;q<1024;q+=256){ int r=q>>5,c=q&31; B2[r*36+c]=dot36(B1,r,B4,c); }
+      __syncthreads();
       #pragma unroll 3
-      for(int q=tid;q<537;q+=256) ((float4*)SB)[q]=((const float4*)pb)[q];
-    }
-  } else {
-    #pragma unroll 3
-    for(int q=tid;q<537;q+=256){ ((float4*)SA)[q]=((const float4*)pa)[q]; ((float4*)SB)[q]=((const float4*)pb)[q]; }
-  }
-  __syncthreads();
-  int fa=(SA[FLGOFF]!=0.f), fb=(SB[FLGOFF]!=0.f);
-  if(mode==1){
-    float* st = out + O_EXXT;
-    #pragma unroll 3
-    for(int q=tid;q<537;q+=256){ ((float4*)st)[q]=((float4*)SB)[q]; ((float4*)pb)[q]=((float4*)SA)[q]; }
-    if(tid==0) pa[FLGOFF]=0.f;
-    return;
-  }
-  if(mode==2){
-    #pragma unroll 3
-    for(int q=tid;q<537;q+=256) ((float4*)pa)[q]=((float4*)SB)[q];
-  }
-  float* X = (mode==2)? SB : SA;  int fx=(mode==2)?fb:fa;
-  float* Y = (mode==2)? SA : SB;  int fy=(mode==2)?fa:fb;
-  if(!fx && !fy){ if(tid==0) pb[FLGOFF]=0.f; return; }
-  if(!fx){ 
-    #pragma unroll 3
-    for(int q=tid;q<537;q+=256) ((float4*)pb)[q]=((float4*)Y)[q]; return; }
-  if(!fy){ 
-    #pragma unroll 3
-    for(int q=tid;q<537;q+=256) ((float4*)pb)[q]=((float4*)X)[q]; return; }
-  #pragma unroll 3
-  for(int q=tid;q<528;q+=256){
-    int r,c; tri_rc(q,r,c);
-    float w = X[QOFF+q] + Y[POFF+q];
-    W[r*36+c]=w; W[c*36+r]=w;
-  }
-  t36_rows(BA, X+ROFF, tid);
-  t36_tr  (BB, Y+ROFF, tid);
-  __syncthreads();
-  double slog = chol_linv36(W, Li, rdg, tid);
-  if(tid<32){
-    float acc=0.f;
-    for(int m=0;m<=tid;++m) acc = fmaf(Li[tid*36+m], X[QQOFF+m]+Y[PPOFF+m], acc);
-    Ls[tid]=acc;
-  }
-  #pragma unroll 4
-  for(int q=tid;q<1024;q+=256){
-    int i2=q>>5, j=q&31;
-    W[j*36+i2] = dot36(Li, i2, BA, j);
-  }
-  __syncthreads();
-  #pragma unroll 4
-  for(int q=tid;q<1024;q+=256){
-    int i2=q>>5, j=q&31;
-    BA[j*36+i2] = dot36(Li, i2, BB, j);
-  }
-  __syncthreads();
-  #pragma unroll 3
-  for(int q=tid;q<528;q+=256){
-    int r,c; tri_rc(q,r,c);
-    pb[POFF+q] = X[POFF+q] - dot36(W, r, W, c);
-    pb[QOFF+q] = Y[QOFF+q] - dot36(BA, r, BA, c);
-  }
-  #pragma unroll 4
-  for(int q=tid;q<1024;q+=256){
-    int r=q>>5, c=q&31;
-    pb[ROFF+q] = -dot36(W, r, BA, c);
-  }
-  if(tid<32){
-    float ap=0.f,aq=0.f;
-    #pragma unroll
-    for(int m=0;m<32;++m){ ap=fmaf(W[tid*36+m],Ls[m],ap); aq=fmaf(BA[tid*36+m],Ls[m],aq); }
-    pb[PPOFF+tid] = X[PPOFF+tid] - ap;
-    pb[QQOFF+tid] = Y[QQOFF+tid] - aq;
-  }
-  if(tid==0){
-    double g = *(double*)(X+GAMOFF) + *(double*)(Y+GAMOFF);
-    double dot=0.0;
-    for(int m=0;m<32;++m) dot += (double)Ls[m]*(double)Ls[m];
-    *(double*)(pb+GAMOFF) = g + 0.5*dot - slog;
-    pb[FLGOFF]=1.f;
-  }
-}
-
-__global__ __launch_bounds__(256,6) void k_point(float* wsf, double* wsd, float* out){
-  __shared__ __align__(16) float SE[2148];
-  __shared__ __align__(16) float W[1152], Li[1152], AUX[1152];
-  __shared__ float rdg[32], uv[32], Lu[32], ev[32], gv[32], yv[32];
-  int tid=threadIdx.x; int b=blockIdx.x;
-  float* base = wsf + F_SCAN;
-  float* outz = out + O_Z;
-  if(b>0){
-    int t = b-1;
-    float* pe = base + (size_t)b*SSTR;
-    #pragma unroll 3
-    for(int q=tid;q<537;q+=256) ((float4*)SE)[q]=((const float4*)pe)[q];
-    if(tid<32) ev[tid]=outz[(size_t)t*32+tid];
-    t36_rows(AUX, wsf+F_LAMA, tid);
-    __syncthreads();
-    #pragma unroll 3
-    for(int q=tid;q<528;q+=256){
-      int r,c; tri_rc(q,r,c);
-      float w = SE[QOFF+q] + wsf[F_ATLAMA + r*32+c] + ((r==c)?1e-6f:0.f);
-      W[r*36+c]=w; W[c*36+r]=w;
-    }
-    if(tid<32) uv[tid]=SE[QQOFF+tid]-wsf[F_ATLAMB+tid];
-    __syncthreads();
-    chol_linv36(W, Li, rdg, tid);
-    if(tid<32){
-      float acc=0.f;
-      for(int m=0;m<=tid;++m) acc=fmaf(Li[tid*36+m],uv[m],acc);
-      Lu[tid]=acc;
-    }
-    #pragma unroll 4
-    for(int q=tid;q<1024;q+=256){
-      int i2=q>>5, j=q&31;
-      W[j*36+i2] = dot36(Li, i2, AUX, j);
-    }
-    __syncthreads();
-    t36_tr36(AUX, Li, tid);
-    if(tid<32){
-      float ag=0.f, ay=0.f;
-      for(int m2=tid;m2<32;++m2){ float lv=Li[m2*36+tid]; ag=fmaf(lv,Lu[m2],ag); ay=fmaf(lv,ev[m2],ay); }
-      gv[tid]=ag; yv[tid]=ay;
-    }
-    __syncthreads();
-    #pragma unroll 4
-    for(int q=tid;q<1024;q+=256){
-      int r=q>>5,c=q&31;
-      pe[BG+q] = dot36(AUX, r, W, c);
-    }
-    float* outc = out + O_CROSS + (size_t)t*1024;
-    #pragma unroll 3
-    for(int q=tid;q<528;q+=256){
-      int r,c; tri_rc(q,r,c);
-      float a = dot36(AUX, r, AUX, c);
-      pe[BP+q]=a; outc[q]=a;
-    }
-    if(tid<32){
-      pe[BCM+tid]=gv[tid]; pe[BCZ+tid]=gv[tid]+yv[tid]; outc[528+tid]=gv[tid];
-    }
-    if(tid==0) pe[FLGOFF]=1.f;
-  } else {
-    const float* st = out + O_EXXT;
-    #pragma unroll 3
-    for(int q=tid;q<537;q+=256) ((float4*)SE)[q]=((const float4*)st)[q];
-    if(tid<32) ev[tid]=outz[(size_t)NN*32+tid];
-    __syncthreads();
-    for(int q=tid;q<528;q+=256){
-      int r,c; tri_rc(q,r,c);
-      float w = SE[QOFF+q] + ((r==c)?1e-6f:0.f);
-      W[r*36+c]=w; W[c*36+r]=w;
-    }
-    if(tid<32) uv[tid]=SE[QQOFF+tid];
-    __syncthreads();
-    double slog2 = chol_linv36(W, Li, rdg, tid);
-    if(tid<32){
-      float acc=0.f;
-      for(int m=0;m<=tid;++m) acc=fmaf(Li[tid*36+m],uv[m],acc);
-      Lu[tid]=acc;
-    }
-    t36_tr36(AUX, Li, tid);
-    __syncthreads();
-    if(tid<32){
-      float am=0.f, ay=0.f;
-      for(int m2=tid;m2<32;++m2){ float lv=Li[m2*36+tid]; am=fmaf(lv,Lu[m2],am); ay=fmaf(lv,ev[m2],ay); }
-      gv[tid]=am; yv[tid]=ay;
-      wsf[F_MLAST+tid]=am; out[O_EX+(size_t)NN*32+tid]=am;
-      float xt=am+ay;
-      wsf[F_XT+tid]=xt; out[O_Z+(size_t)NN*32+tid]=xt;
-    }
-    __syncthreads();
-    for(int q=tid;q<1024;q+=256){
-      int r=q>>5,c=q&31;
-      float a = dot36(AUX, r, AUX, c);
-      wsf[F_COVT+q]=a;
-      out[O_EXXT+(size_t)NN*1024+q]=a+gv[r]*gv[c];
-    }
-    if(tid==0){
-      double gam=*(const double*)(SE+GAMOFF);
-      double hm=0.0;
-      for(int m=0;m<32;++m) hm += (double)uv[m]*(double)gv[m];
-      wsd[WSD_LOGZQ] = gam + 0.5*hm + 0.5*Dd*LOG2PI_ - slog2;
-    }
-  }
-}
-
-__device__ __forceinline__ int amap(int j){ return (j<NN)? (NN-j) : 0; }
-
-__global__ __launch_bounds__(256,4) void k_ca(float* wsf, int d, int mode){
-  __shared__ __align__(16) float SA[2148], SB[2148];
-  __shared__ __align__(16) float GY36[1152], GB[1152], PX36[1152];
-  int tid = threadIdx.x;
-  int i = blockIdx.x;
-  int iA = (i<<(d+1)) + (1<<d) - 1;
-  int iB = iA + (1<<d);
-  float* base = wsf + F_SCAN;
-  float* pa = base + (size_t)amap(iA)*SSTR;
-  float* pb = base + (size_t)amap(iB)*SSTR;
-  #pragma unroll 3
-  for(int q=tid;q<537;q+=256){ ((float4*)SA)[q]=((const float4*)pa)[q]; ((float4*)SB)[q]=((const float4*)pb)[q]; }
-  __syncthreads();
-  int fa=(SA[FLGOFF]!=0.f), fb=(SB[FLGOFF]!=0.f);
-  if(mode==1){
-    #pragma unroll 3
-    for(int q=tid;q<537;q+=256) ((float4*)pb)[q]=((float4*)SA)[q];
-    if(tid==0) pa[FLGOFF]=0.f;
-    return;
-  }
-  if(mode==2){
-    #pragma unroll 3
-    for(int q=tid;q<537;q+=256) ((float4*)pa)[q]=((float4*)SB)[q];
-  }
-  float* X = (mode==2)? SB : SA;  int fx=(mode==2)?fb:fa;
-  float* Y = (mode==2)? SA : SB;  int fy=(mode==2)?fa:fb;
-  if(!fx && !fy){ if(tid==0) pb[FLGOFF]=0.f; return; }
-  if(!fx){ 
-    #pragma unroll 3
-    for(int q=tid;q<537;q+=256) ((float4*)pb)[q]=((float4*)Y)[q]; return; }
-  if(!fy){ 
-    #pragma unroll 3
-    for(int q=tid;q<537;q+=256) ((float4*)pb)[q]=((float4*)X)[q]; return; }
-  t36_rows(GY36, Y+BG, tid);
-  t36_tr  (GB,   X+BG, tid);
-  t36_sym (PX36, X+BP, tid);
-  __syncthreads();
-  #pragma unroll 4
-  for(int q=tid;q<1024;q+=256){
-    int r=q>>5,c=q&31;
-    pb[BG+q] = dot36(GY36, r, GB, c);
-  }
-  __syncthreads();
-  #pragma unroll 4
-  for(int q=tid;q<1024;q+=256){
-    int r=q>>5,c=q&31;
-    GB[r*36+c] = dot36(GY36, r, PX36, c);
-  }
-  __syncthreads();
-  #pragma unroll 3
-  for(int q=tid;q<528;q+=256){
-    int r,c; tri_rc(q,r,c);
-    pb[BP+q] = dot36(GB, r, GY36, c) + Y[BP+q];
-  }
-  if(tid<32){
-    float az=0.f,am=0.f;
-    #pragma unroll
-    for(int m=0;m<32;++m){ float g=GY36[tid*36+m]; az=fmaf(g,X[BCZ+m],az); am=fmaf(g,X[BCM+m],am); }
-    pb[BCZ+tid]=az+Y[BCZ+tid];
-    pb[BCM+tid]=am+Y[BCM+tid];
-  }
-  if(tid==0) pb[FLGOFF]=1.f;
-}
-
-__global__ __launch_bounds__(256,6) void k_smz(float* wsf, float* out){
-  __shared__ __align__(16) float G36[1152], CV36[1152], Tm36[1152];
-  __shared__ float mlv[32], xtv[32], mv[32], zv[32];
-  int tid=threadIdx.x;
-  int t = blockIdx.x;
-  const float* pe = wsf + F_SCAN + (size_t)t*SSTR;
-  t36_rows(G36,  pe+BG,       tid);
-  t36_rows(CV36, wsf+F_COVT,  tid);
-  if(tid<32){ mlv[tid]=wsf[F_MLAST+tid]; xtv[tid]=wsf[F_XT+tid]; }
-  __syncthreads();
-  if(tid<32){
-    float am=0.f, az=0.f;
-    #pragma unroll
-    for(int m=0;m<32;++m){
-      float g=G36[tid*36+m];
-      am=fmaf(g, mlv[m], am);
-      az=fmaf(g, xtv[m], az);
-    }
-    mv[tid]=am+pe[BCM+tid];
-    zv[tid]=az+pe[BCZ+tid];
-    out[O_EX+(size_t)t*32+tid]=mv[tid];
-    out[O_Z +(size_t)t*32+tid]=zv[tid];
-  }
-  #pragma unroll 4
-  for(int q=tid;q<1024;q+=256){
-    int r=q>>5,c=q&31;
-    Tm36[r*36+c] = dot36(G36, r, CV36, c);
-  }
-  __syncthreads();
-  #pragma unroll 3
-  for(int q=tid;q<528;q+=256){
-    int r,c; tri_rc(q,r,c);
-    float cov = dot36(Tm36, r, G36, c) + pe[BP+q];
-    float e = cov + mv[r]*mv[c];
-    out[O_EXXT+(size_t)t*1024 + r*32+c]=e;
-    if(r!=c) out[O_EXXT+(size_t)t*1024 + c*32+r]=e;
+      for(int q=tid;q<528;q+=256){
+        int r,c; tri_rc(q,r,c);
+        float e2 = dot36(B2,r,B1,c) + C[BP+q] + mv[r]*mv[c];
+        out[O_EXXT+(size_t)t*1024 + r*32+c]=e2;
+        if(r!=c) out[O_EXXT+(size_t)t*1024 + c*32+r]=e2;
+      }
+    }
+    int s=(j<NN)? (NN-j) : 0;
+    ld_slot(Y, wsf + F_SCAN + (size_t)s*SSTR, tid);
+    comb_a(C, Y, B1,B2,B3,B4, vcz,vcm, tid);
   }
 }
 
@@ -949,14 +1055,20 @@
   k_hmmpow<<<1,256,0,stream>>>(tl, wsf);
   k_hmmab<<<32,256,0,stream>>>(il, wsf);
   k_cat<<<128,256,0,stream>>>(tl, wsf, out);
-  for(int d=0; d<13; ++d) k_cf<<<(8192>>(d+1)),256,0,stream>>>(rJ, rh, wsf, wsd, out, d, 0);
-  k_cf<<<1,256,0,stream>>>(rJ, rh, wsf, wsd, out, 12, 1);
-  for(int d=11; d>=0; --d) k_cf<<<(8192>>(d+1)),256,0,stream>>>(rJ, rh, wsf, wsd, out, d, 2);
-  k_point<<<8192,256,0,stream>>>(wsf, wsd, out);
-  for(int d=0; d<13; ++d) k_ca<<<(8192>>(d+1)),256,0,stream>>>(wsf, d, 0);
-  k_ca<<<1,256,0,stream>>>(wsf, 12, 1);
-  for(int d=11; d>=0; --d) k_ca<<<(8192>>(d+1)),256,0,stream>>>(wsf, d, 2);
-  k_smz<<<NN,256,0,stream>>>(wsf, out);
+  kf_agg<<<1024,256,0,stream>>>(rJ, rh, wsf, wsd, out);
+  kf_seq<<<128,256,0,stream>>>(out, SAGG0, SSUP0);
+  kf_seq<<<16,256,0,stream>>>(out, SSUP0, SHYP0);
+  kf_sqx<<<1,256,0,stream>>>(out, SHYP0, 16);
+  kf_sqp<<<16,256,0,stream>>>(out, SHYP0, SSUP0);
+  kf_sqp<<<128,256,0,stream>>>(out, SSUP0, SAGG0);
+  kf_prop<<<1024,256,0,stream>>>(rJ, rh, wsf, wsd, out);
+  ka_agg<<<1024,256,0,stream>>>(wsf, out);
+  ka_seq<<<128,256,0,stream>>>(out, SAGG0, SSUP0);
+  ka_seq<<<16,256,0,stream>>>(out, SSUP0, SHYP0);
+  ka_sqx<<<1,256,0,stream>>>(out, SHYP0, 16);
+  ka_sqp<<<16,256,0,stream>>>(out, SHYP0, SSUP0);
+  ka_sqp<<<128,256,0,stream>>>(out, SSUP0, SAGG0);
+  ka_prop<<<1024,256,0,stream>>>(wsf, out);
   k_cross<<<NN,256,0,stream>>>(wsf, out);
   k_terms<<<1024,256,0,stream>>>(rJ, rh, plam, wsf, wsd, out);
   k_final<<<1,256,0,stream>>>(il, tl, ilp, tlp, ptau, wsf, wsd, out);
```

New measurement: 2.920 ms. 1.41x slower.
